# Optimization experiments

Hardware: AMD Instinct MI355X
Metric: run time of the kernel (lower is better)

The kernel has to match this reference:

```python
import jax, jax.numpy as jnp
import numpy as np

LEAK = 0.2

def leaky(x):
    return jnp.where(x > 0, x, LEAK * x)

def relu(x):
    return jnp.maximum(x, 0)

def conv1d(x, w):
    # x [B,Cin,L], w [Cout,Cin,3], stride 1, padding 1
    return jax.lax.conv_general_dilated(x, w, (1,), [(1, 1)],
        dimension_numbers=('NCH', 'OIH', 'NCH'))

def conv2d(x, w, pad, dil=1, groups=1):
    return jax.lax.conv_general_dilated(x, w, (1, 1), [(pad, pad), (pad, pad)],
        rhs_dilation=(dil, dil), feature_group_count=groups,
        dimension_numbers=('NCHW', 'OIHW', 'NCHW'))

def bn2d(x, p, eps=1e-5):
    # p: [4,C] = gamma, beta, running_mean, running_var (eval-mode BN)
    g, b, m, v = p
    s = (1, -1, 1, 1)
    return (x - m.reshape(s)) * (g.reshape(s) / jnp.sqrt(v.reshape(s) + eps)) + b.reshape(s)

def layernorm(x, g, b, eps=1e-5):
    mu = x.mean(-1, keepdims=True)
    var = ((x - mu) ** 2).mean(-1, keepdims=True)
    return (x - mu) / jnp.sqrt(var + eps) * g + b

def l2n(x, axis, eps):
    n = jnp.sqrt((x * x).sum(axis, keepdims=True))
    return x / jnp.maximum(n, eps)


def setup_inputs() -> dict:
    key = jax.random.key(0)
    B, C, H, W = 4, 64, 48, 48
    D, Fn, T, V = 256, 8, 4, 16
    E = 16  # orthogonal prototype embed dim
    ks = iter(jax.random.split(key, 64))
    def rn(shape, s=0.05):
        return jax.random.normal(next(ks), shape, jnp.float32) * s
    def bnp(c):
        return jnp.stack([1.0 + rn((c,), 0.1), rn((c,), 0.1), rn((c,), 0.1), 1.0 + jnp.abs(rn((c,), 0.1))])
    return dict(
        basis_vector_bank=jax.random.normal(next(ks), (T, V, D), jnp.float32),
        task_f=jax.random.normal(next(ks), (B, C, 16, 16), jnp.float32),
        img_f=jax.random.normal(next(ks), (B, C, H, W), jnp.float32),
        protos=jax.random.normal(next(ks), (T, E), jnp.float32),
        tA_w1=rn((E // 4, 1, 3)), tA_w2=rn((E // 2, E // 4, 3)),
        iA_w=rn((E // 2, C, 3, 3)), iA_bn=bnp(E // 2),
        at_w1=rn((E, Fn // 2 * E)), at_b1=rn((Fn // 2 * E,)),
        at_ln_g=jnp.ones((Fn // 2 * E,)), at_ln_b=jnp.zeros((Fn // 2 * E,)),
        at_w2=rn((Fn // 2 * E, Fn * E)), at_b2=rn((Fn * E,)),
        bv_t1=rn((D // 4, 1, 3)), bv_t2=rn((D // 2, D // 4, 3)),
        bv_ic1=rn((D // 4, C, 3, 3)), bv_bn1=bnp(D // 4),
        bv_ic2=rn((D // 2, D // 4, 3, 3)), bv_bn2=bnp(D // 2),
        bv_w1=rn((D, D // 4)), bv_b1=rn((D // 4,)),
        bv_ln_g=jnp.ones((D // 4,)), bv_ln_b=jnp.zeros((D // 4,)),
        bv_w2=rn((D // 4, D)), bv_b2=rn((D,)),
        m1_w1=rn((D, D // 4)), m1_b1=rn((D // 4,)),
        m1_ln_g=jnp.ones((D // 4,)), m1_ln_b=jnp.zeros((D // 4,)),
        m1_w2=rn((D // 4, C * C)), m1_b2=rn((C * C,)),
        m3_w1=rn((D, D // 4)), m3_b1=rn((D // 4,)),
        m3_ln_g=jnp.ones((D // 4,)), m3_ln_b=jnp.zeros((D // 4,)),
        m3_w2=rn((D // 4, 9 * C * C)), m3_b2=rn((9 * C * C,)),
        blr_bn=bnp(C),
        zc_w=rn((C, C, 1, 1), 0.01), zc_b=rn((C,), 0.01),
    )


def _forward(basis_vector_bank, task_f, img_f, protos, tA_w1, tA_w2, iA_w, iA_bn,
             at_w1, at_b1, at_ln_g, at_ln_b, at_w2, at_b2,
             bv_t1, bv_t2, bv_ic1, bv_bn1, bv_ic2, bv_bn2,
             bv_w1, bv_b1, bv_ln_g, bv_ln_b, bv_w2, bv_b2,
             m1_w1, m1_b1, m1_ln_g, m1_ln_b, m1_w2, m1_b2,
             m3_w1, m3_b1, m3_ln_g, m3_ln_b, m3_w2, m3_b2,
             blr_bn, zc_w, zc_b):
    T, V, D = basis_vector_bank.shape
    B, C, H, W = img_f.shape
    E = protos.shape[1]
    Fn = at_w2.shape[1] // E
    tau = 0.5

    # --- A2SI routing features ---
    xt = task_f.reshape(B, 1, -1)
    t1 = conv1d(leaky(conv1d(xt, tA_w1)), tA_w2).mean(-1)          # [B,E/2]
    i1 = leaky(bn2d(conv2d(img_f, iA_w, 1), iA_bn)).mean((2, 3))   # [B,E/2]
    f1 = jnp.concatenate([t1, i1], axis=1)                         # [B,E]
    h = relu(layernorm(f1 @ at_w1 + at_b1, at_ln_g, at_ln_b))
    tif = (h @ at_w2 + at_b2).reshape(B, E, Fn)                    # [B,E,F]
    logits = jnp.einsum('te,bef->bft', l2n(protos, -1, 1e-8), l2n(tif, 1, 1e-8))  # [B,F,T]

    # hard gumbel-softmax (straight-through), fixed noise key for determinism
    u = jax.random.uniform(jax.random.key(42), logits.shape, jnp.float32, 1e-10, 1.0)
    g = -jnp.log(-jnp.log(u))
    y = jax.nn.softmax((logits + g) / tau, axis=-1)
    idx = jnp.argmax(y, axis=-1)                                   # [B,F]
    y_hard = jax.nn.one_hot(idx, T, dtype=y.dtype)
    set_type = y_hard + y - jax.lax.stop_gradient(y)

    bank_flat = basis_vector_bank.reshape(T, V * D)
    sbvb = jnp.einsum('bft,tk->bfk', set_type, bank_flat).reshape(B, Fn, V, D)

    # --- BasisV_filter: filter feature ---
    xt2 = task_f.reshape(B, C, -1)
    rms = jnp.sqrt((xt2 ** 2).mean((1, 2), keepdims=True))
    xt2 = (xt2 / (rms + 1e-8)).reshape(B, 1, -1)
    te = conv1d(leaky(conv1d(xt2, bv_t1)), bv_t2).mean(-1)         # [B,D/2]
    ie = leaky(bn2d(conv2d(img_f, bv_ic1, 1), bv_bn1))
    ie = leaky(bn2d(conv2d(ie, bv_ic2, 1), bv_bn2)).mean((2, 3))   # [B,D/2]
    ff = jnp.concatenate([te, ie], axis=1)                         # [B,D]
    ff = relu(layernorm(ff @ bv_w1 + bv_b1, bv_ln_g, bv_ln_b)) @ bv_w2 + bv_b2

    # --- per-(batch,type) group gather/top-k/scatter, vectorized ---
    # group bank = bank of first filter with that type (hard one-hot -> type's bank)
    occ = idx[:, None, :] == jnp.arange(T)[None, :, None]          # [B,T,F]
    first = jnp.argmax(occ, axis=-1)                               # [B,T]
    Bg = jnp.take_along_axis(sbvb, first[:, :, None, None], axis=1)  # [B,T,V,D]
    # all rows of Q within a group are identical (filter_f expanded over F),
    # so S.max(0) == cosine(ff[b], Bg[b,t])
    scores = jnp.einsum('bd,btvd->btv', l2n(ff, -1, 1e-12), l2n(Bg, -1, 1e-12))
    order = jnp.argsort(-scores, axis=-1)                          # [B,T,V] topk order
    lt = jnp.tril(jnp.ones((Fn, Fn), bool), -1)                    # j < i
    rank = ((idx[:, :, None] == idx[:, None, :]) & lt).sum(-1)     # position in group
    bidx = jnp.arange(B)[:, None]
    sel = order[bidx, idx, rank]                                   # [B,F]
    bvf = Bg[bidx, idx, sel]                                       # [B,F,D]

    # --- per-filter dynamic convolutions ---
    w1 = relu(layernorm(bvf @ m1_w1 + m1_b1, m1_ln_g, m1_ln_b)) @ m1_w2 + m1_b2
    w1 = w1.reshape(B, Fn, C, C)                                   # [B,F,out,in]
    w3 = relu(layernorm(bvf @ m3_w1 + m3_b1, m3_ln_g, m3_ln_b)) @ m3_w2 + m3_b2
    w3 = w3.reshape(B * Fn, C, C, 3, 3)

    dp0 = jnp.einsum('bfoc,bchw->bfohw', w1, img_f)                # 1x1 branch
    xin = jnp.broadcast_to(img_f[:, None], (B, Fn, C, H, W)).reshape(1, B * Fn * C, H, W)
    ker = w3.reshape(B * Fn * C, C, 3, 3)
    dpd = [conv2d(xin, ker, d, dil=d, groups=B * Fn).reshape(B, Fn, C, H, W)
           for d in (1, 2, 3)]                                     # same-padded dilated 3x3
    t_ = idx[:, :, None, None, None]
    dp = jnp.where(t_ == 0, dp0, jnp.where(t_ == 1, dpd[0],
         jnp.where(t_ == 2, dpd[1], dpd[2])))                      # [B,F,C,H,W]

    x = leaky(bn2d(dp.reshape(B * Fn, C, H, W), blr_bn)).reshape(B, Fn, C, H, W).mean(1)
    a = conv2d(x, zc_w, 0) + zc_b.reshape(1, -1, 1, 1)
    return a + img_f


@jax.jit
def reference(basis_vector_bank, task_f, img_f, protos, tA_w1, tA_w2, iA_w, iA_bn,
              at_w1, at_b1, at_ln_g, at_ln_b, at_w2, at_b2,
              bv_t1, bv_t2, bv_ic1, bv_bn1, bv_ic2, bv_bn2,
              bv_w1, bv_b1, bv_ln_g, bv_ln_b, bv_w2, bv_b2,
              m1_w1, m1_b1, m1_ln_g, m1_ln_b, m1_w2, m1_b2,
              m3_w1, m3_b1, m3_ln_g, m3_ln_b, m3_w2, m3_b2,
              blr_bn, zc_w, zc_b):
    return _forward(basis_vector_bank, task_f, img_f, protos, tA_w1, tA_w2, iA_w, iA_bn,
                    at_w1, at_b1, at_ln_g, at_ln_b, at_w2, at_b2,
                    bv_t1, bv_t2, bv_ic1, bv_bn1, bv_ic2, bv_bn2,
                    bv_w1, bv_b1, bv_ln_g, bv_ln_b, bv_w2, bv_b2,
                    m1_w1, m1_b1, m1_ln_g, m1_ln_b, m1_w2, m1_b2,
                    m3_w1, m3_b1, m3_ln_g, m3_ln_b, m3_w2, m3_b2,
                    blr_bn, zc_w, zc_b)
```

## Files before the change

### kernel.cpp

```cpp
#include <hip/hip_runtime.h>
#include <math.h>

#define LEAKC 0.2f

#define NB 4
#define NC 64
#define LLEN 16384
#define HW 2304
#define PP 54
#define PHW 2916
#define SLABP 72
#define CP 72
#define IE1C 50

typedef __attribute__((ext_vector_type(8))) short short8;
typedef __attribute__((ext_vector_type(4))) float floatx4;

__device__ __forceinline__ float leaky(float x){ return x > 0.f ? x : LEAKC*x; }

__device__ __forceinline__ float wave_sum64(float v){
  for(int off=32;off;off>>=1) v += __shfl_xor(v,off);
  return v;
}

__device__ __forceinline__ unsigned short f2bf(float x){
  unsigned u=__float_as_uint(x);
  unsigned r=u+0x7FFFu+((u>>16)&1u);
  return (unsigned short)(r>>16);
}

__device__ __forceinline__ void threefry2x32(unsigned k0, unsigned k1, unsigned& x0, unsigned& x1){
  unsigned ks0=k0, ks1=k1, ks2=k0^k1^0x1BD11BDAu;
  x0+=ks0; x1+=ks1;
  const int rot0[4]={13,15,26,6};
  const int rot1[4]={17,29,16,24};
#define TF_APPLY(rr) {for(int r=0;r<4;r++){x0+=x1; x1=(x1<<rr[r])|(x1>>(32-rr[r])); x1^=x0;}}
  TF_APPLY(rot0); x0+=ks1; x1+=ks2+1u;
  TF_APPLY(rot1); x0+=ks2; x1+=ks0+2u;
  TF_APPLY(rot0); x0+=ks0; x1+=ks1+3u;
  TF_APPLY(rot1); x0+=ks1; x1+=ks2+4u;
  TF_APPLY(rot0); x0+=ks2; x1+=ks0+5u;
#undef TF_APPLY
}

__device__ __forceinline__ float jax_uniform128(int i){
  unsigned x0=0u, x1=(unsigned)i;
  threefry2x32(0u,42u,x0,x1);
  unsigned bits = x0 ^ x1;
  unsigned fb=(bits>>9)|0x3f800000u;
  float f=__uint_as_float(fb)-1.0f;
  float u=f*(1.0f-1e-10f)+1e-10f;
  return fmaxf(1e-10f,u);
}

__global__ __launch_bounds__(256) void k_pre(const float* __restrict__ task_f,
                      const float* __restrict__ w1A, const float* __restrict__ w1B,
                      float* __restrict__ totApart, float* __restrict__ a0A, float* __restrict__ aLA,
                      float* __restrict__ totBpart, float* __restrict__ a0B, float* __restrict__ aLB,
                      float* __restrict__ rmspart,
                      const float* __restrict__ img,
                      const float* __restrict__ w1, const float* __restrict__ w2,
                      const float* __restrict__ wa,
                      unsigned short* __restrict__ imgTP,
                      unsigned short* __restrict__ W1T, unsigned short* __restrict__ W2T,
                      unsigned short* __restrict__ WAT,
                      const float* __restrict__ mw1, const float* __restrict__ mw3,
                      const float* __restrict__ bvw1p, const float* __restrict__ bvw2p,
                      const float* __restrict__ bvt2p, const float* __restrict__ atw2p,
                      const float* __restrict__ bankp, float* __restrict__ warm){
  if(blockIdx.x<256){
    int b=blockIdx.x>>6, seg=blockIdx.x&63;
    const float* x=task_f+b*LLEN;
    float tA[4]={0,0,0,0};
    float tB[64];
#pragma unroll
    for(int c=0;c<64;c++) tB[c]=0.f;
    float sq=0.f;
    int l=seg*256+threadIdx.x;
    {
      float xm=(l>0)?x[l-1]:0.f;
      float xc=x[l];
      float xp=(l<LLEN-1)?x[l+1]:0.f;
      sq=xc*xc;
#pragma unroll
      for(int c=0;c<4;c++){
        float a=leaky(w1A[c*3+0]*xm + w1A[c*3+1]*xc + w1A[c*3+2]*xp);
        tA[c]=a;
        if(l==0) a0A[b*4+c]=a;
        if(l==LLEN-1) aLA[b*4+c]=a;
      }
#pragma unroll
      for(int c=0;c<64;c++){
        float a=leaky(w1B[c*3+0]*xm + w1B[c*3+1]*xc + w1B[c*3+2]*xp);
        tB[c]=a;
        if(l==0) a0B[b*64+c]=a;
        if(l==LLEN-1) aLB[b*64+c]=a;
      }
    }
    sq=wave_sum64(sq);
#pragma unroll
    for(int c=0;c<4;c++) tA[c]=wave_sum64(tA[c]);
#pragma unroll
    for(int c=0;c<64;c++){
      float v=tB[c];
      for(int off=32;off;off>>=1) v+=__shfl_down(v,off);
      tB[c]=v;
    }
    __shared__ float redB[4][64];
    __shared__ float redA[4][4];
    __shared__ float redQ[4];
    int wave=threadIdx.x>>6, lane=threadIdx.x&63;
    if(lane==0){
#pragma unroll
      for(int c=0;c<64;c++) redB[wave][c]=tB[c];
#pragma unroll
      for(int c=0;c<4;c++) redA[wave][c]=tA[c];
      redQ[wave]=sq;
    }
    __syncthreads();
    if(threadIdx.x<64){
      float s=redB[0][threadIdx.x]+redB[1][threadIdx.x]+redB[2][threadIdx.x]+redB[3][threadIdx.x];
      totBpart[(size_t)(b*64+seg)*64+threadIdx.x]=s;
    } else if(threadIdx.x<68){
      int c=threadIdx.x-64;
      totApart[(b*64+seg)*4+c]=redA[0][c]+redA[1][c]+redA[2][c]+redA[3][c];
    } else if(threadIdx.x==68){
      rmspart[b*64+seg]=redQ[0]+redQ[1]+redQ[2]+redQ[3];
    }
  } else if(blockIdx.x<400){
    int blk=blockIdx.x-256;
    int b=blk/36, t=blk%36;
    int p0=t*64;
    __shared__ float tile[64][65];
    int pp=threadIdx.x&63, c4=threadIdx.x>>6;
    for(int r=0;r<16;r++){
      int c=c4*16+r;
      tile[c][pp]=img[(b*64+c)*HW + p0+pp];
    }
    __syncthreads();
    int pxl=threadIdx.x>>2, cg=(threadIdx.x&3)*16;
    unsigned out[8];
#pragma unroll
    for(int q=0;q<8;q++){
      unsigned lo=f2bf(tile[cg+2*q][pxl]);
      unsigned hi=f2bf(tile[cg+2*q+1][pxl]);
      out[q]=lo|(hi<<16);
    }
    int px=p0+pxl;
    int h=px/48, w=px-h*48;
    int poff=(h+3)*PP+(w+3);
    unsigned* dst=(unsigned*)(imgTP + ((size_t)(b*PHW+poff))*64 + cg);
#pragma unroll
    for(int q=0;q<8;q++) dst[q]=out[q];
  } else if(blockIdx.x<868){
    int n=(blockIdx.x-400)*256+threadIdx.x;
    if(n<9*64*64){
      int tap=n>>12, oc=(n>>6)&63, c=n&63;
      W1T[n]=f2bf(w1[oc*576+c*9+tap]);
    } else if(n<9*64*64+9*128*64){
      int m=n-9*64*64;
      int tap=m/8192, r=m-tap*8192, oc=r>>6, c=r&63;
      W2T[m]=f2bf(w2[oc*576+c*9+tap]);
    } else {
      int q=n-9*64*64-9*128*64;
      if(q<9*16*64){
        int tap=q>>10, r=q&1023, o=r>>6, c=r&63;
        WAT[q]=(o<8)?f2bf(wa[o*576+c*9+tap]):(unsigned short)0;
      }
    }
  } else if(blockIdx.x<884){
    int t=(blockIdx.x-868)*256+threadIdx.x;
    float a=0.f;
    for(int i=t;i*16<16384;i+=4096) a+=mw1[i*16];
    for(int i=t;i*16<16384;i+=4096) a+=mw3[i*16];
    for(int i=t;i*16<16384;i+=4096) a+=bvw1p[i*16];
    for(int i=t;i*16<16384;i+=4096) a+=bvw2p[i*16];
    for(int i=t;i*16<24576;i+=4096) a+=bvt2p[i*16];
    for(int i=t;i*16<8192;i+=4096) a+=atw2p[i*16];
    for(int i=t;i*16<16384;i+=4096) a+=bankp[i*16];
    warm[t&1023]=a;
  } else {
    int id=(blockIdx.x-884)*256+threadIdx.x;
    uint4 z=make_uint4(0,0,0,0);
    for(int cch=id;cch<19584;cch+=4096){
      int ck=cch&7, pxid=cch>>3;
      int b=pxid/612, p=pxid-b*612;
      int h,w;
      if(p<324){ int r=p/54; w=p-r*54; h=(r<3)?r:(r+48); }
      else { int q=p-324; int r2=q/6; int cc=q-r2*6; h=3+r2; w=(cc<3)?cc:(cc+48); }
      *(uint4*)(imgTP + ((size_t)(b*PHW + h*PP + w))*64 + ck*8)=z;
    }
  }
}

__global__ __launch_bounds__(512) void k_conv12(const unsigned short* __restrict__ imgTP,
                        const unsigned short* __restrict__ W1T,
                        const unsigned short* __restrict__ W2T,
                        const unsigned short* __restrict__ WAT,
                        const float* __restrict__ bn1, const float* __restrict__ bn2,
                        const float* __restrict__ bnA,
                        float* __restrict__ iepart, float* __restrict__ i1part){
  int tid=threadIdx.x;
  int lane=tid&63, wv=tid>>6;
  int n0=lane&15, kg=lane>>4;
  if(blockIdx.x<96){
    int blk=blockIdx.x;
    int b=blk/24, hp=blk-b*24;
    int h0=hp*2;
    __shared__ unsigned short slab[6*54*SLABP];
    __shared__ unsigned short ie1[4*IE1C*CP];
    {
      const unsigned short* ibase=imgTP+((size_t)b*PHW+(size_t)(h0+1)*PP)*64;
      for(int e=tid;e<6*54*8;e+=512){
        int rr=e/(54*8), rem=e-rr*54*8, w=rem>>3, ck=rem&7;
        uint4 v=*(const uint4*)(ibase+((size_t)(rr*PP+w))*64+ck*8);
        *(uint4*)(slab+(rr*54+w)*SLABP+ck*8)=v;
      }
      if(tid<64){
        int br=tid>>4, cq=(tid>>3)&1, ck=tid&7;
        *(uint4*)(ie1+((size_t)(br*IE1C+(cq?49:0)))*CP+ck*8)=make_uint4(0,0,0,0);
      }
    }
    __syncthreads();
    {
      int mt=wv&3, rh=wv>>2;
      floatx4 acc[2][3];
#pragma unroll
      for(int rr=0;rr<2;rr++)
#pragma unroll
        for(int nt=0;nt<3;nt++) acc[rr][nt]=(floatx4){0.f,0.f,0.f,0.f};
#pragma unroll
      for(int ti=0;ti<3;ti++){
#pragma unroll
        for(int tj=0;tj<3;tj++){
          int tap=ti*3+tj;
          const unsigned short* Ab=W1T+(size_t)tap*4096;
#pragma unroll
          for(int c0=0;c0<64;c0+=32){
            short8 a=*(const short8*)(Ab+((mt*16+n0)*64+c0+kg*8));
#pragma unroll
            for(int rr=0;rr<2;rr++){
              int sr=rh*2+rr+ti;
#pragma unroll
              for(int nt=0;nt<3;nt++){
                int sc=nt*16+n0+tj+2;
                short8 bv=*(const short8*)(slab+(sr*54+sc)*SLABP+c0+kg*8);
                acc[rr][nt]=__builtin_amdgcn_mfma_f32_16x16x32_bf16(a,bv,acc[rr][nt],0,0,0);
              }
            }
          }
        }
      }
      int obase=mt*16+kg*4;
      float scale[4],m_[4],be_[4];
#pragma unroll
      for(int reg=0;reg<4;reg++){
        int o=obase+reg;
        scale[reg]=bn1[o]/sqrtf(bn1[192+o]+1e-5f);
        m_[reg]=bn1[128+o]; be_[reg]=bn1[64+o];
      }
#pragma unroll
      for(int rr=0;rr<2;rr++){
        int br=rh*2+rr;
        bool rv=((unsigned)(h0-1+br))<48u;
#pragma unroll
        for(int nt=0;nt<3;nt++){
          float v0=rv?leaky((acc[rr][nt][0]-m_[0])*scale[0]+be_[0]):0.f;
          float v1=rv?leaky((acc[rr][nt][1]-m_[1])*scale[1]+be_[1]):0.f;
          float v2=rv?leaky((acc[rr][nt][2]-m_[2])*scale[2]+be_[2]):0.f;
          float v3=rv?leaky((acc[rr][nt][3]-m_[3])*scale[3]+be_[3]):0.f;
          unsigned w0=f2bf(v0)|((unsigned)f2bf(v1)<<16);
          unsigned w1=f2bf(v2)|((unsigned)f2bf(v3)<<16);
          uint2 pk={w0,w1};
          *(uint2*)(ie1+((size_t)(br*IE1C+(nt*16+1+n0)))*CP+obase)=pk;
        }
      }
    }
    __syncthreads();
    {
      int mt2=wv;
      floatx4 acc[6];
#pragma unroll
      for(int i=0;i<6;i++) acc[i]=(floatx4){0.f,0.f,0.f,0.f};
#pragma unroll
      for(int ti=0;ti<3;ti++){
#pragma unroll
        for(int tj=0;tj<3;tj++){
          int tap=ti*3+tj;
          const unsigned short* Ab=W2T+(size_t)tap*8192;
#pragma unroll
          for(int c0=0;c0<64;c0+=32){
            short8 a=*(const short8*)(Ab+((mt2*16+n0)*64+c0+kg*8));
#pragma unroll
            for(int rr=0;rr<2;rr++){
              int sr=rr+ti;
#pragma unroll
              for(int wc=0;wc<3;wc++){
                int q=wc*16+n0+tj;
                short8 bv=*(const short8*)(ie1+((size_t)(sr*IE1C+q))*CP+c0+kg*8);
                acc[rr*3+wc]=__builtin_amdgcn_mfma_f32_16x16x32_bf16(a,bv,acc[rr*3+wc],0,0,0);
              }
            }
          }
        }
      }
      int obase=mt2*16+kg*4;
#pragma unroll
      for(int reg=0;reg<4;reg++){
        int o=obase+reg;
        float scale=bn2[o]/sqrtf(bn2[384+o]+1e-5f);
        float m_=bn2[256+o], be_=bn2[128+o];
        float part=0;
#pragma unroll
        for(int i=0;i<6;i++) part+=leaky((acc[i][reg]-m_)*scale+be_);
        for(int off=1;off<16;off<<=1) part+=__shfl_xor(part,off);
        if(n0==0) iepart[(b*24+hp)*128+o]=part*(1.f/2304.f);
      }
    }
  } else {
    int blk2=blockIdx.x-96;
    int b=blk2/3, hg=blk2-b*3;
    int hp=hg*8+wv;
    int h0=hp*2;
    const unsigned short* ib=imgTP+(size_t)b*PHW*64;
    floatx4 acc[6];
#pragma unroll
    for(int i=0;i<6;i++) acc[i]=(floatx4){0.f,0.f,0.f,0.f};
#pragma unroll
    for(int ti=0;ti<3;ti++){
#pragma unroll
      for(int tj=0;tj<3;tj++){
        int tap=ti*3+tj;
        const unsigned short* Ab=WAT+(size_t)tap*1024;
#pragma unroll
        for(int c0=0;c0<64;c0+=32){
          short8 a=*(const short8*)(Ab+(n0*64+c0+kg*8));
#pragma unroll
          for(int rr=0;rr<2;rr++){
            int r=h0+rr+ti-1+3;
#pragma unroll
            for(int wc=0;wc<3;wc++){
              int w=wc*16+n0+tj-1+3;
              short8 bv=*(const short8*)(ib+((size_t)(r*PP+w)*64+c0+kg*8));
              acc[rr*3+wc]=__builtin_amdgcn_mfma_f32_16x16x32_bf16(a,bv,acc[rr*3+wc],0,0,0);
            }
          }
        }
      }
    }
    int obase=kg*4;
#pragma unroll
    for(int reg=0;reg<4;reg++){
      int o=obase+reg;
      float part=0;
      if(o<8){
        float scale=bnA[o]/sqrtf(bnA[24+o]+1e-5f);
        float m_=bnA[16+o], be_=bnA[8+o];
#pragma unroll
        for(int i=0;i<6;i++) part+=leaky((acc[i][reg]-m_)*scale+be_);
      }
      for(int off=1;off<16;off<<=1) part+=__shfl_xor(part,off);
      if(n0==0 && o<8) i1part[(b*24+hp)*8+o]=part*(1.f/2304.f);
    }
  }
}

__global__ __launch_bounds__(512,1) void k_mid(
    const float* __restrict__ totApart, const float* __restrict__ a0A, const float* __restrict__ aLA,
    const float* __restrict__ totBpart, const float* __restrict__ a0B, const float* __restrict__ aLB,
    const float* __restrict__ rmspart,
    const float* __restrict__ tA_w2, const float* __restrict__ bv_t2,
    const float* __restrict__ i1part, const float* __restrict__ iepart,
    const float* __restrict__ at_w1, const float* __restrict__ at_b1,
    const float* __restrict__ at_ln_g, const float* __restrict__ at_ln_b,
    const float* __restrict__ at_w2, const float* __restrict__ at_b2,
    const float* __restrict__ protos,
    const float* __restrict__ bv_w1, const float* __restrict__ bv_b1,
    const float* __restrict__ bv_ln_g, const float* __restrict__ bv_ln_b,
    const float* __restrict__ bv_w2, const float* __restrict__ bv_b2,
    const float* __restrict__ bank,
    const float* __restrict__ m1_w1, const float* __restrict__ m1_b1,
    const float* __restrict__ m1_g,  const float* __restrict__ m1_bb,
    const float* __restrict__ m3_w1, const float* __restrict__ m3_b1,
    const float* __restrict__ m3_g,  const float* __restrict__ m3_bb,
    int* __restrict__ idxo, float* __restrict__ hid1, float* __restrict__ hid3){
  int b=blockIdx.x;
  int tid=threadIdx.x;
  int lane=tid&63, wv=tid>>6;
  const float invL=1.0f/16384.0f;
  __shared__ float sT[64], s0[64], sL[64];
  __shared__ float totA_s[4];
  __shared__ float rms_s;
  __shared__ float part[512];
  __shared__ float te_s[128], t1_s[8];
  __shared__ float f1[16], h[64], tif[128], tifn[128], tden[8], pden[4], pn[64], z[32];
  __shared__ int sidx[8], sfirst[4], srank[8], rows[8];
  __shared__ float fbuf[256], hh[64], ffn_s[256], finv_s;
  __shared__ float scores[64];
  __shared__ int order[64];
  __shared__ float bvf[2048];

  if(tid<64){
    float s=0;
#pragma unroll 8
    for(int seg=0;seg<64;seg++) s+=totBpart[(size_t)(b*64+seg)*64+tid];
    sT[tid]=s;
  } else if(tid<128){
    int t=tid-64;
    s0[t]=a0B[b*64+t]; sL[t]=aLB[b*64+t];
  } else if(tid<192){
    float v=rmspart[b*64+(tid-128)];
    v=wave_sum64(v);
    if(tid==128) rms_s=v;
  } else if(tid<256){
    int c=tid-192;
    if(c<4){
      float s=0;
#pragma unroll 8
      for(int seg=0;seg<64;seg++) s+=totApart[(b*64+seg)*4+c];
      totA_s[c]=s;
    }
  }
  __syncthreads();
  float scB=1.0f/(sqrtf(rms_s*invL)+1e-8f);
  if(tid<256){
    int c2=tid&127, h2=tid>>7;
    const float* wr=bv_t2+c2*192;
    float s=0;
    for(int c1=h2*32;c1<h2*32+32;c1+=8){
      float4 q[6];
      const float4* r4=(const float4*)(wr+c1*3);
#pragma unroll
      for(int u=0;u<6;u++) q[u]=r4[u];
      const float* qq=(const float*)q;
#pragma unroll
      for(int u=0;u<8;u++){
        int c=c1+u;
        float T=sT[c], A0=s0[c], AL=sL[c];
        s += qq[u*3+0]*(T-AL) + qq[u*3+1]*T + qq[u*3+2]*(T-A0);
      }
    }
    part[tid]=s;
  } else if(tid>=384 && tid<392){
    int c2=tid-384;
    float s=0;
    for(int c1=0;c1<4;c1++){
      float T=totA_s[c1], A0=a0A[b*4+c1], AL=aLA[b*4+c1];
      const float* w=&tA_w2[(c2*4+c1)*3];
      s += w[0]*(T-AL) + w[1]*T + w[2]*(T-A0);
    }
    t1_s[c2]=s*invL;
  }
  __syncthreads();
  if(tid<128) te_s[tid]=(part[tid]+part[tid+128])*invL*scB;
  __syncthreads();

  if(tid<8) f1[tid]=t1_s[tid];
  else if(tid<16){
    int f=tid-8;
    float s=0;
#pragma unroll
    for(int g=0;g<24;g++) s+=i1part[(b*24+g)*8+f];
    f1[tid]=s;
  }
  __syncthreads();
  if(tid<64){
    float s=at_b1[lane];
#pragma unroll
    for(int i=0;i<16;i++) s+=f1[i]*at_w1[i*64+lane];
    float mu=wave_sum64(s)*(1.f/64.f);
    float d=s-mu;
    float var=wave_sum64(d*d)*(1.f/64.f);
    h[lane]=fmaxf(d*(1.0f/sqrtf(var+1e-5f))*at_ln_g[lane]+at_ln_b[lane],0.f);
  }
  __syncthreads();
  if(tid<256){
    int n=tid&127, h2=tid>>7;
    float a0=0,a1=0;
    for(int k=h2*32;k<h2*32+32;k+=2){
      a0+=h[k]*at_w2[k*128+n];
      a1+=h[k+1]*at_w2[(k+1)*128+n];
    }
    part[tid]=a0+a1;
  }
  __syncthreads();
  if(tid<128) tif[tid]=at_b2[tid]+part[tid]+part[tid+128];
  __syncthreads();
  if(tid<8){
    int f=tid;
    float ss=0; for(int e=0;e<16;e++){float v=tif[e*8+f]; ss+=v*v;}
    tden[f]=fmaxf(sqrtf(ss),1e-8f);
  } else if(tid<12){
    int t=tid-8;
    float ss=0; for(int e=0;e<16;e++){float v=protos[t*16+e]; ss+=v*v;}
    pden[t]=fmaxf(sqrtf(ss),1e-8f);
  }
  __syncthreads();
  if(tid<128) tifn[tid]=tif[tid]/tden[tid&7];
  if(tid<64) pn[tid]=protos[tid]/pden[tid>>4];
  __syncthreads();
  if(tid<32){
    int f=tid>>2, t=tid&3;
    float ss=0;
#pragma unroll
    for(int e=0;e<16;e++) ss+=pn[t*16+e]*tifn[e*8+f];
    float u=jax_uniform128(b*32+f*4+t);
    float g=-logf(-logf(u));
    z[tid]=ss+g;
  }
  __syncthreads();
  if(tid<8){
    float best=z[tid*4]; int bi=0;
    for(int t=1;t<4;t++){ float v=z[tid*4+t]; if(v>best){best=v;bi=t;} }
    sidx[tid]=bi;
  }
  __syncthreads();
  if(tid<4){
    int t=tid;
    int fi=0;
    for(int f=7;f>=0;f--) if(sidx[f]==t) fi=f;
    sfirst[t]=fi;
  } else if(tid<12){
    int f=tid-4;
    int c=0; for(int f2=0;f2<f;f2++) if(sidx[f2]==sidx[f]) c++;
    srank[f]=c;
  }
  __syncthreads();

  if(tid<128) fbuf[tid]=te_s[tid];
  else if(tid<256){
    int c=tid-128;
    float s=0;
#pragma unroll 8
    for(int g=0;g<24;g++) s+=iepart[(b*24+g)*128+c];
    fbuf[tid]=s;
  }
  __syncthreads();
  if(tid<256){
    int l64=tid&63, q=tid>>6;
    float a0=0,a1=0,a2=0,a3=0;
    for(int k=q*64;k<q*64+64;k+=4){
      a0+=fbuf[k]  *bv_w1[k*64+l64];
      a1+=fbuf[k+1]*bv_w1[(k+1)*64+l64];
      a2+=fbuf[k+2]*bv_w1[(k+2)*64+l64];
      a3+=fbuf[k+3]*bv_w1[(k+3)*64+l64];
    }
    part[tid]=((a0+a1)+(a2+a3));
  }
  __syncthreads();
  if(tid<64){
    float s=bv_b1[lane]+part[lane]+part[64+lane]+part[128+lane]+part[192+lane];
    float mu=wave_sum64(s)*(1.f/64.f);
    float d=s-mu;
    float var=wave_sum64(d*d)*(1.f/64.f);
    hh[lane]=fmaxf(d*(1.0f/sqrtf(var+1e-5f))*bv_ln_g[lane]+bv_ln_b[lane],0.f);
  }
  __syncthreads();
  {
    int n=tid&255, h2=tid>>8;
    float a0=0,a1=0;
    for(int k=h2*32;k<h2*32+32;k+=2){
      a0+=hh[k]*bv_w2[k*256+n];
      a1+=hh[k+1]*bv_w2[(k+1)*256+n];
    }
    part[tid]=a0+a1;
  }
  __syncthreads();
  if(tid<256) ffn_s[tid]=bv_b2[tid]+part[tid]+part[tid+256];
  __syncthreads();
  if(tid<64){
    float sq=0;
#pragma unroll
    for(int u=0;u<4;u++){ float v=ffn_s[u*64+lane]; sq+=v*v; }
    sq=wave_sum64(sq);
    if(lane==0) finv_s=1.0f/fmaxf(sqrtf(sq),1e-12f);
  }
  __syncthreads();
  if(tid<256) ffn_s[tid]*=finv_s;
  __syncthreads();

  if(tid<128){
    int it=tid&63, h2=tid>>6;
    int t=it>>4, v=it&15;
    int tt=sidx[sfirst[t]];
    const float4* row=(const float4*)(bank+(tt*16+v)*256);
    float sa=0,na=0;
    for(int d4=h2*32;d4<h2*32+32;d4++){
      float4 r=row[d4];
      const float* fp=&ffn_s[d4*4];
      sa+=fp[0]*r.x+fp[1]*r.y+fp[2]*r.z+fp[3]*r.w;
      na+=r.x*r.x+r.y*r.y+r.z*r.z+r.w*r.w;
    }
    part[tid]=sa;
    part[256+tid]=na;
  }
  __syncthreads();
  if(tid<64) scores[tid]=(part[tid]+part[tid+64])/fmaxf(sqrtf(part[256+tid]+part[320+tid]),1e-12f);
  __syncthreads();
  if(tid<4){
    const float* sc=&scores[tid*16];
    unsigned used=0;
    for(int pk=0;pk<16;pk++){
      int best=-1; float bv=-1e30f;
      for(int v2=0;v2<16;v2++){
        if(used&(1u<<v2)) continue;
        float vv=sc[v2];
        if(best<0||vv>bv){bv=vv;best=v2;}
      }
      used|=1u<<best;
      order[tid*16+pk]=best;
    }
  }
  __syncthreads();
  if(tid<8){
    int t=sidx[tid];
    int v=order[t*16+srank[tid]];
    rows[tid]=t*16+v;
    idxo[b*8+tid]=t;
  }
  __syncthreads();

  for(int ii=tid;ii<2048;ii+=512){
    int r=ii>>8, d=ii&255;
    bvf[ii]=bank[rows[r]*256+d];
  }
  __syncthreads();
  {
    int r=wv;
    const float* bp=&bvf[r*256];
    float a0=0,a1=0,a2=0,a3=0;
    float c0=0,c1=0,c2=0,c3=0;
    for(int d=0;d<256;d+=4){
      float b0=bp[d],b1=bp[d+1],b2=bp[d+2],b3=bp[d+3];
      a0+=b0*m1_w1[d*64+lane];
      a1+=b1*m1_w1[(d+1)*64+lane];
      a2+=b2*m1_w1[(d+2)*64+lane];
      a3+=b3*m1_w1[(d+3)*64+lane];
      c0+=b0*m3_w1[d*64+lane];
      c1+=b1*m3_w1[(d+1)*64+lane];
      c2+=b2*m3_w1[(d+2)*64+lane];
      c3+=b3*m3_w1[(d+3)*64+lane];
    }
    float s1=m1_b1[lane]+((a0+a1)+(a2+a3));
    float s3=m3_b1[lane]+((c0+c1)+(c2+c3));
    float mu=wave_sum64(s1)*(1.f/64.f);
    float dd=s1-mu;
    float var=wave_sum64(dd*dd)*(1.f/64.f);
    hid1[(b*8+r)*64+lane]=fmaxf(dd*(1.0f/sqrtf(var+1e-5f))*m1_g[lane]+m1_bb[lane],0.f);
    mu=wave_sum64(s3)*(1.f/64.f);
    dd=s3-mu;
    var=wave_sum64(dd*dd)*(1.f/64.f);
    hid3[(b*8+r)*64+lane]=fmaxf(dd*(1.0f/sqrtf(var+1e-5f))*m3_g[lane]+m3_bb[lane],0.f);
  }
}

__global__ __launch_bounds__(256) void k_heads(const float* __restrict__ hid1, const float* __restrict__ hid3,
                        const float* __restrict__ w2a, const float* __restrict__ b2a,
                        const float* __restrict__ w2b, const float* __restrict__ b2b,
                        unsigned short* __restrict__ A1, unsigned short* __restrict__ A3){
  __shared__ float hl[2048];
  if(blockIdx.x<16){
    int n=blockIdx.x*256+threadIdx.x;
    for(int i=threadIdx.x;i<2048;i+=256) hl[i]=hid1[i];
    __syncthreads();
    float wcol[64];
#pragma unroll
    for(int k=0;k<64;k++) wcol[k]=w2a[k*4096+n];
    float bb=b2a[n];
    for(int bf=0;bf<32;bf++){
      float s=bb;
#pragma unroll
      for(int k=0;k<64;k++) s+=hl[bf*64+k]*wcol[k];
      A1[bf*4096+n]=f2bf(s);
    }
  } else {
    int n=(blockIdx.x-16)*256+threadIdx.x;
    for(int i=threadIdx.x;i<2048;i+=256) hl[i]=hid3[i];
    __syncthreads();
    float wcol[64];
#pragma unroll
    for(int k=0;k<64;k++) wcol[k]=w2b[(size_t)k*36864+n];
    float bb=b2b[n];
    int o=n/576, rem=n-o*576;
    int c=rem/9, tap=rem-c*9;
    size_t base=((size_t)tap*64+o)*64+c;
    for(int bf=0;bf<32;bf++){
      float s=bb;
#pragma unroll
      for(int k=0;k<64;k++) s+=hl[bf*64+k]*wcol[k];
      A3[(size_t)bf*9*4096+base]=f2bf(s);
    }
  }
}

__global__ __launch_bounds__(512) void k_dynF(const unsigned short* __restrict__ imgTP,
                       const unsigned short* __restrict__ A1, const unsigned short* __restrict__ A3,
                       const int* __restrict__ idx, const float* __restrict__ bn,
                       const float* __restrict__ zc_w, const float* __restrict__ zc_b,
                       const float* __restrict__ img, float* __restrict__ out){
  int blk=blockIdx.x;
  int b=blk/48, r0=blk-b*48;
  int tid=threadIdx.x;
  int lane=tid&63, w8=tid>>6;
  int mt=w8&3, fh=w8>>2;
  int n0=lane&15, kg=lane>>4;
  __shared__ unsigned short slab[7*54*SLABP];
  __shared__ float xl[64*50];
  __shared__ float zl[4096];
  for(int i=tid;i<4096;i+=512) zl[i]=zc_w[i];
  for(int i=tid;i<3200;i+=512) xl[i]=0.f;
  {
    const unsigned short* ibase=imgTP+((size_t)b*PHW+(size_t)r0*PP)*64;
    for(int e=tid;e<7*54*8;e+=512){
      int rr=e/(54*8), rem=e-rr*54*8, w=rem>>3, ck=rem&7;
      uint4 v=*(const uint4*)(ibase + ((size_t)(rr*PP+w))*64 + ck*8);
      *(uint4*)(slab + (rr*54+w)*SLABP + ck*8)=v;
    }
  }
  __syncthreads();
  int obase=mt*16+kg*4;
  float scale[4],m_[4],be_[4];
#pragma unroll
  for(int reg=0;reg<4;reg++){
    int o=obase+reg;
    scale[reg]=bn[o]/sqrtf(bn[192+o]+1e-5f);
    m_[reg]=bn[128+o]; be_[reg]=bn[64+o];
  }
  float xsum[3][4];
#pragma unroll
  for(int wc=0;wc<3;wc++)
#pragma unroll
    for(int reg=0;reg<4;reg++) xsum[wc][reg]=0.f;
  for(int f=fh*4;f<fh*4+4;f++){
    int bf=b*8+f;
    int tt=idx[bf];
    floatx4 acc[3];
#pragma unroll
    for(int i=0;i<3;i++) acc[i]=(floatx4){0.f,0.f,0.f,0.f};
    if(tt==0){
      const unsigned short* Ab=A1+(size_t)bf*4096;
#pragma unroll
      for(int c0=0;c0<64;c0+=32){
        short8 a=*(const short8*)(Ab+((mt*16+n0)*64+c0+kg*8));
#pragma unroll
        for(int wc=0;wc<3;wc++){
          short8 bv=*(const short8*)(slab + (3*54 + wc*16+n0+3)*SLABP + c0+kg*8);
          acc[wc]=__builtin_amdgcn_mfma_f32_16x16x32_bf16(a,bv,acc[wc],0,0,0);
        }
      }
    } else {
      int d=tt;
      const unsigned short* A3b=A3+(size_t)bf*9*4096;
#pragma unroll
      for(int ti=0;ti<3;ti++){
        int lr=d*(ti-1)+3;
#pragma unroll
        for(int tj=0;tj<3;tj++){
          int tap=ti*3+tj;
          int dw=d*(tj-1)+3;
          const unsigned short* Ab=A3b+(size_t)tap*4096;
#pragma unroll
          for(int c0=0;c0<64;c0+=32){
            short8 a=*(const short8*)(Ab+((mt*16+n0)*64+c0+kg*8));
#pragma unroll
            for(int wc=0;wc<3;wc++){
              short8 bv=*(const short8*)(slab + (lr*54 + wc*16+n0+dw)*SLABP + c0+kg*8);
              acc[wc]=__builtin_amdgcn_mfma_f32_16x16x32_bf16(a,bv,acc[wc],0,0,0);
            }
          }
        }
      }
    }
#pragma unroll
    for(int wc=0;wc<3;wc++)
#pragma unroll
      for(int reg=0;reg<4;reg++)
        xsum[wc][reg]+=leaky((acc[wc][reg]-m_[reg])*scale[reg]+be_[reg]);
  }
#pragma unroll
  for(int wc=0;wc<3;wc++)
#pragma unroll
    for(int reg=0;reg<4;reg++)
      atomicAdd(&xl[(obase+reg)*50 + wc*16+n0], xsum[wc][reg]*0.125f);
  __syncthreads();
  size_t base=(size_t)b*64*HW + r0*48;
  for(int e=tid;e<3072;e+=512){
    int o=e/48, px=e-o*48;
    float s=zc_b[o];
#pragma unroll
    for(int c=0;c<64;c++) s+=zl[o*64+c]*xl[c*50+px];
    size_t a=base+(size_t)o*HW+px;
    out[a]=s+img[a];
  }
}

extern "C" void kernel_launch(void* const* d_in, const int* in_sizes, int n_in,
                              void* d_out, int out_size, void* d_ws, size_t ws_size,
                              hipStream_t stream){
  const float* bank   =(const float*)d_in[0];
  const float* task_f =(const float*)d_in[1];
  const float* img_f  =(const float*)d_in[2];
  const float* protos =(const float*)d_in[3];
  const float* tA_w1  =(const float*)d_in[4];
  const float* tA_w2  =(const float*)d_in[5];
  const float* iA_w   =(const float*)d_in[6];
  const float* iA_bn  =(const float*)d_in[7];
  const float* at_w1  =(const float*)d_in[8];
  const float* at_b1  =(const float*)d_in[9];
  const float* at_ln_g=(const float*)d_in[10];
  const float* at_ln_b=(const float*)d_in[11];
  const float* at_w2  =(const float*)d_in[12];
  const float* at_b2  =(const float*)d_in[13];
  const float* bv_t1  =(const float*)d_in[14];
  const float* bv_t2  =(const float*)d_in[15];
  const float* bv_ic1 =(const float*)d_in[16];
  const float* bv_bn1 =(const float*)d_in[17];
  const float* bv_ic2 =(const float*)d_in[18];
  const float* bv_bn2 =(const float*)d_in[19];
  const float* bv_w1  =(const float*)d_in[20];
  const float* bv_b1  =(const float*)d_in[21];
  const float* bv_ln_g=(const float*)d_in[22];
  const float* bv_ln_b=(const float*)d_in[23];
  const float* bv_w2  =(const float*)d_in[24];
  const float* bv_b2  =(const float*)d_in[25];
  const float* m1_w1  =(const float*)d_in[26];
  const float* m1_b1  =(const float*)d_in[27];
  const float* m1_ln_g=(const float*)d_in[28];
  const float* m1_ln_b=(const float*)d_in[29];
  const float* m1_w2  =(const float*)d_in[30];
  const float* m1_b2  =(const float*)d_in[31];
  const float* m3_w1  =(const float*)d_in[32];
  const float* m3_b1  =(const float*)d_in[33];
  const float* m3_ln_g=(const float*)d_in[34];
  const float* m3_ln_b=(const float*)d_in[35];
  const float* m3_w2  =(const float*)d_in[36];
  const float* m3_b2  =(const float*)d_in[37];
  const float* blr_bn =(const float*)d_in[38];
  const float* zc_w   =(const float*)d_in[39];
  const float* zc_b   =(const float*)d_in[40];

  float* ws=(float*)d_ws;
  float* totApart=ws+0;
  float* a0A  =ws+1024;
  float* aLA  =ws+1040;
  float* totBpart=ws+1056;
  float* a0B  =ws+17440;
  float* aLB  =ws+17696;
  float* rmspart=ws+17952;
  float* i1part =ws+18208;
  float* iepart =ws+18976;
  int*   idxp   =(int*)(ws+31264);
  float* hid1=ws+31296;
  float* hid3=ws+33344;
  unsigned short* A1p  =(unsigned short*)(ws+35392);
  unsigned short* A3p  =(unsigned short*)(ws+100928);
  unsigned short* imgTP=(unsigned short*)(ws+690752);
  unsigned short* W1Tp =(unsigned short*)(ws+1064000);
  unsigned short* W2Tp =(unsigned short*)(ws+1082432);
  unsigned short* WATp =(unsigned short*)(ws+1119296);
  float* warm =ws+1123904;

  k_pre<<<900,256,0,stream>>>(task_f, tA_w1, bv_t1,
                              totApart, a0A, aLA, totBpart, a0B, aLB, rmspart,
                              img_f, bv_ic1, bv_ic2, iA_w, imgTP, W1Tp, W2Tp, WATp,
                              m1_w1, m3_w1, bv_w1, bv_w2, bv_t2, at_w2, bank, warm);
  k_conv12<<<108,512,0,stream>>>(imgTP, W1Tp, W2Tp, WATp, bv_bn1, bv_bn2, iA_bn,
                                 iepart, i1part);
  k_mid<<<4,512,0,stream>>>(totApart,a0A,aLA,totBpart,a0B,aLB, rmspart, tA_w2, bv_t2,
                            i1part, iepart,
                            at_w1, at_b1, at_ln_g, at_ln_b, at_w2, at_b2, protos,
                            bv_w1, bv_b1, bv_ln_g, bv_ln_b, bv_w2, bv_b2, bank,
                            m1_w1, m1_b1, m1_ln_g, m1_ln_b,
                            m3_w1, m3_b1, m3_ln_g, m3_ln_b,
                            idxp, hid1, hid3);
  k_heads<<<160,256,0,stream>>>(hid1, hid3, m1_w2, m1_b2, m3_w2, m3_b2, A1p, A3p);
  k_dynF<<<192,512,0,stream>>>(imgTP, A1p, A3p, idxp, blr_bn, zc_w, zc_b, img_f, (float*)d_out);

  (void)in_sizes; (void)n_in; (void)out_size; (void)ws_size;
}
```

Before: 267.2 us.

## Merge five kernels into two with in-kernel flag-based dependency gating

Folds the preprocessing and conv12 stages into one kernel (kA), and the mid, heads and dynamic-filter stages into another (kB). Dependencies between stages are enforced with global-memory release/acquire flags and spin-waits instead of kernel boundaries. Consumer blocks can start loading their slabs before producer results are ready, which removes launch gaps and lets tail work overlap. The spin-waits assume the producer blocks are resident or already scheduled, so they risk deadlock if occupancy is insufficient, and waiting blocks hold CU resources while they spin.

```diff
diff --git a/kernel.cpp b/kernel.cpp
--- a/kernel.cpp
+++ b/kernel.cpp
@@ -12,6 +12,7 @@
 #define SLABP 72
 #define CP 72
 #define IE1C 50
+#define MAGIC 0x1357ACE9
 
 typedef __attribute__((ext_vector_type(8))) short short8;
 typedef __attribute__((ext_vector_type(4))) float floatx4;
@@ -53,30 +54,72 @@
   return fmaxf(1e-10f,u);
 }
 
-__global__ __launch_bounds__(256) void k_pre(const float* __restrict__ task_f,
-                      const float* __restrict__ w1A, const float* __restrict__ w1B,
-                      float* __restrict__ totApart, float* __restrict__ a0A, float* __restrict__ aLA,
-                      float* __restrict__ totBpart, float* __restrict__ a0B, float* __restrict__ aLB,
-                      float* __restrict__ rmspart,
-                      const float* __restrict__ img,
-                      const float* __restrict__ w1, const float* __restrict__ w2,
-                      const float* __restrict__ wa,
-                      unsigned short* __restrict__ imgTP,
-                      unsigned short* __restrict__ W1T, unsigned short* __restrict__ W2T,
-                      unsigned short* __restrict__ WAT,
-                      const float* __restrict__ mw1, const float* __restrict__ mw3,
-                      const float* __restrict__ bvw1p, const float* __restrict__ bvw2p,
-                      const float* __restrict__ bvt2p, const float* __restrict__ atw2p,
-                      const float* __restrict__ bankp, float* __restrict__ warm){
-  if(blockIdx.x<256){
-    int b=blockIdx.x>>6, seg=blockIdx.x&63;
+__device__ __forceinline__ void gate_slots(int* slots, int nsl, int tid){
+  if(tid<nsl){
+    while(__hip_atomic_load(&slots[tid], __ATOMIC_ACQUIRE, __HIP_MEMORY_SCOPE_AGENT)!=MAGIC)
+      __builtin_amdgcn_s_sleep(8);
+  }
+  __syncthreads();
+}
+
+__device__ __forceinline__ void mark_slot(int* slot, int tid){
+  __syncthreads();
+  if(tid==0) __hip_atomic_store(slot, MAGIC, __ATOMIC_RELEASE, __HIP_MEMORY_SCOPE_AGENT);
+}
+
+__device__ __forceinline__ void gate_cnt(int* cnt, int target, int tid){
+  if(tid==0){
+    while(__hip_atomic_load(cnt, __ATOMIC_ACQUIRE, __HIP_MEMORY_SCOPE_AGENT)<target)
+      __builtin_amdgcn_s_sleep(8);
+  }
+  __syncthreads();
+}
+
+struct MidSM {
+  float sT[64], s0[64], sL[64];
+  float totA_s[4]; float rms_s;
+  float part[512];
+  float te_s[128], t1_s[8];
+  float f1[16], h[64], tif[128], tifn[128], tden[8], pden[4], pn[64], z[32];
+  int sidx[8], sfirst[4], srank[8], rows[8];
+  float fbuf[256], hh[64], ffn_s[256], finv_s;
+  float scores[64];
+  int order[64];
+  float bvf[2048];
+};
+
+__global__ __launch_bounds__(512) void kA(
+    const float* __restrict__ task_f,
+    const float* __restrict__ w1A, const float* __restrict__ w1B,
+    float* __restrict__ totApart, float* __restrict__ a0A, float* __restrict__ aLA,
+    float* __restrict__ totBpart, float* __restrict__ a0B, float* __restrict__ aLB,
+    float* __restrict__ rmspart,
+    const float* __restrict__ img,
+    const float* __restrict__ w1, const float* __restrict__ w2, const float* __restrict__ wa,
+    unsigned short* __restrict__ imgTP,
+    unsigned short* __restrict__ W1T, unsigned short* __restrict__ W2T, unsigned short* __restrict__ WAT,
+    const float* __restrict__ mw1, const float* __restrict__ mw3,
+    const float* __restrict__ bvw1p, const float* __restrict__ bvw2p,
+    const float* __restrict__ bvt2p, const float* __restrict__ atw2p,
+    const float* __restrict__ bankp, float* __restrict__ warm,
+    const float* __restrict__ bn1, const float* __restrict__ bn2, const float* __restrict__ bnA,
+    float* __restrict__ iepart, float* __restrict__ i1part,
+    int* __restrict__ slotA, int* __restrict__ bflags){
+  __shared__ __align__(16) char smraw[75456];
+  int tid=threadIdx.x;
+  int lane=tid&63, wv=tid>>6;
+  int n0=lane&15, kg=lane>>4;
+  int blk=blockIdx.x;
+
+  if(blk<128){
+    int b=blk>>5, half=tid>>8, seg=(blk&31)*2+half, t256=tid&255;
     const float* x=task_f+b*LLEN;
     float tA[4]={0,0,0,0};
     float tB[64];
 #pragma unroll
     for(int c=0;c<64;c++) tB[c]=0.f;
     float sq=0.f;
-    int l=seg*256+threadIdx.x;
+    int l=seg*256+t256;
     {
       float xm=(l>0)?x[l-1]:0.f;
       float xc=x[l];
@@ -106,39 +149,39 @@
       for(int off=32;off;off>>=1) v+=__shfl_down(v,off);
       tB[c]=v;
     }
-    __shared__ float redB[4][64];
-    __shared__ float redA[4][4];
-    __shared__ float redQ[4];
-    int wave=threadIdx.x>>6, lane=threadIdx.x&63;
+    float (*redB)[64]=(float(*)[64])smraw;
+    float (*redA)[4]=(float(*)[4])(smraw+2048);
+    float *redQ=(float*)(smraw+2048+128);
     if(lane==0){
 #pragma unroll
-      for(int c=0;c<64;c++) redB[wave][c]=tB[c];
-#pragma unroll
-      for(int c=0;c<4;c++) redA[wave][c]=tA[c];
-      redQ[wave]=sq;
-    }
-    __syncthreads();
-    if(threadIdx.x<64){
-      float s=redB[0][threadIdx.x]+redB[1][threadIdx.x]+redB[2][threadIdx.x]+redB[3][threadIdx.x];
-      totBpart[(size_t)(b*64+seg)*64+threadIdx.x]=s;
-    } else if(threadIdx.x<68){
-      int c=threadIdx.x-64;
-      totApart[(b*64+seg)*4+c]=redA[0][c]+redA[1][c]+redA[2][c]+redA[3][c];
-    } else if(threadIdx.x==68){
-      rmspart[b*64+seg]=redQ[0]+redQ[1]+redQ[2]+redQ[3];
-    }
-  } else if(blockIdx.x<400){
-    int blk=blockIdx.x-256;
-    int b=blk/36, t=blk%36;
+      for(int c=0;c<64;c++) redB[wv][c]=tB[c];
+#pragma unroll
+      for(int c=0;c<4;c++) redA[wv][c]=tA[c];
+      redQ[wv]=sq;
+    }
+    __syncthreads();
+    int w0=half*4;
+    if(t256<64){
+      float s=redB[w0][t256]+redB[w0+1][t256]+redB[w0+2][t256]+redB[w0+3][t256];
+      totBpart[(size_t)(b*64+seg)*64+t256]=s;
+    } else if(t256<68){
+      int c=t256-64;
+      totApart[(b*64+seg)*4+c]=redA[w0][c]+redA[w0+1][c]+redA[w0+2][c]+redA[w0+3][c];
+    } else if(t256==68){
+      rmspart[b*64+seg]=redQ[w0]+redQ[w0+1]+redQ[w0+2]+redQ[w0+3];
+    }
+  } else if(blk<200){
+    int j=blk-128, b=j/18, pr=j-b*18, half=tid>>8, t=pr*2+half, t256=tid&255;
+    float (*tile2)[64][65]=(float(*)[64][65])smraw;
+    float (*tile)[65]=tile2[half];
     int p0=t*64;
-    __shared__ float tile[64][65];
-    int pp=threadIdx.x&63, c4=threadIdx.x>>6;
+    int pp=t256&63, c4=t256>>6;
     for(int r=0;r<16;r++){
       int c=c4*16+r;
       tile[c][pp]=img[(b*64+c)*HW + p0+pp];
     }
     __syncthreads();
-    int pxl=threadIdx.x>>2, cg=(threadIdx.x&3)*16;
+    int pxl=t256>>2, cg=(t256&3)*16;
     unsigned out[8];
 #pragma unroll
     for(int q=0;q<8;q++){
@@ -152,24 +195,25 @@
     unsigned* dst=(unsigned*)(imgTP + ((size_t)(b*PHW+poff))*64 + cg);
 #pragma unroll
     for(int q=0;q<8;q++) dst[q]=out[q];
-  } else if(blockIdx.x<868){
-    int n=(blockIdx.x-400)*256+threadIdx.x;
-    if(n<9*64*64){
-      int tap=n>>12, oc=(n>>6)&63, c=n&63;
-      W1T[n]=f2bf(w1[oc*576+c*9+tap]);
-    } else if(n<9*64*64+9*128*64){
-      int m=n-9*64*64;
-      int tap=m/8192, r=m-tap*8192, oc=r>>6, c=r&63;
-      W2T[m]=f2bf(w2[oc*576+c*9+tap]);
-    } else {
-      int q=n-9*64*64-9*128*64;
-      if(q<9*16*64){
+    mark_slot(&slotA[j], tid);
+  } else if(blk<230){
+    for(int n=(blk-200)*512+tid;n<119808;n+=15360){
+      if(n<36864){
+        int tap=n>>12, oc=(n>>6)&63, c=n&63;
+        W1T[n]=f2bf(w1[oc*576+c*9+tap]);
+      } else if(n<110592){
+        int m=n-36864;
+        int tap=m/8192, r=m-tap*8192, oc=r>>6, c=r&63;
+        W2T[m]=f2bf(w2[oc*576+c*9+tap]);
+      } else {
+        int q=n-110592;
         int tap=q>>10, r=q&1023, o=r>>6, c=r&63;
         WAT[q]=(o<8)?f2bf(wa[o*576+c*9+tap]):(unsigned short)0;
       }
     }
-  } else if(blockIdx.x<884){
-    int t=(blockIdx.x-868)*256+threadIdx.x;
+    mark_slot(&slotA[72+(blk-200)], tid);
+  } else if(blk<238){
+    int t=(blk-230)*512+tid;
     float a=0.f;
     for(int i=t;i*16<16384;i+=4096) a+=mw1[i*16];
     for(int i=t;i*16<16384;i+=4096) a+=mw3[i*16];
@@ -179,8 +223,10 @@
     for(int i=t;i*16<8192;i+=4096) a+=atw2p[i*16];
     for(int i=t;i*16<16384;i+=4096) a+=bankp[i*16];
     warm[t&1023]=a;
-  } else {
-    int id=(blockIdx.x-884)*256+threadIdx.x;
+  } else if(blk<246){
+    int hb=blk-238;
+    if(hb==0 && tid<2) __hip_atomic_store(&bflags[tid],0,__ATOMIC_RELAXED,__HIP_MEMORY_SCOPE_AGENT);
+    int id=hb*512+tid;
     uint4 z=make_uint4(0,0,0,0);
     for(int cch=id;cch<19584;cch+=4096){
       int ck=cch&7, pxid=cch>>3;
@@ -190,25 +236,14 @@
       else { int q=p-324; int r2=q/6; int cc=q-r2*6; h=3+r2; w=(cc<3)?cc:(cc+48); }
       *(uint4*)(imgTP + ((size_t)(b*PHW + h*PP + w))*64 + ck*8)=z;
     }
-  }
-}
-
-__global__ __launch_bounds__(512) void k_conv12(const unsigned short* __restrict__ imgTP,
-                        const unsigned short* __restrict__ W1T,
-                        const unsigned short* __restrict__ W2T,
-                        const unsigned short* __restrict__ WAT,
-                        const float* __restrict__ bn1, const float* __restrict__ bn2,
-                        const float* __restrict__ bnA,
-                        float* __restrict__ iepart, float* __restrict__ i1part){
-  int tid=threadIdx.x;
-  int lane=tid&63, wv=tid>>6;
-  int n0=lane&15, kg=lane>>4;
-  if(blockIdx.x<96){
-    int blk=blockIdx.x;
-    int b=blk/24, hp=blk-b*24;
+    mark_slot(&slotA[102+hb], tid);
+  } else if(blk<342){
+    gate_slots(slotA,110,tid);
+    int cblk=blk-246;
+    int b=cblk/24, hp=cblk-b*24;
     int h0=hp*2;
-    __shared__ unsigned short slab[6*54*SLABP];
-    __shared__ unsigned short ie1[4*IE1C*CP];
+    unsigned short* slab=(unsigned short*)smraw;
+    unsigned short* ie1=(unsigned short*)(smraw+46656);
     {
       const unsigned short* ibase=imgTP+((size_t)b*PHW+(size_t)(h0+1)*PP)*64;
       for(int e=tid;e<6*54*8;e+=512){
@@ -270,8 +305,8 @@
           float v2=rv?leaky((acc[rr][nt][2]-m_[2])*scale[2]+be_[2]):0.f;
           float v3=rv?leaky((acc[rr][nt][3]-m_[3])*scale[3]+be_[3]):0.f;
           unsigned w0=f2bf(v0)|((unsigned)f2bf(v1)<<16);
-          unsigned w1=f2bf(v2)|((unsigned)f2bf(v3)<<16);
-          uint2 pk={w0,w1};
+          unsigned w1p=f2bf(v2)|((unsigned)f2bf(v3)<<16);
+          uint2 pk={w0,w1p};
           *(uint2*)(ie1+((size_t)(br*IE1C+(nt*16+1+n0)))*CP+obase)=pk;
         }
       }
@@ -318,8 +353,9 @@
       }
     }
   } else {
-    int blk2=blockIdx.x-96;
-    int b=blk2/3, hg=blk2-b*3;
+    gate_slots(slotA,110,tid);
+    int ablk=blk-342;
+    int b=ablk/3, hg=ablk%3;
     int hp=hg*8+wv;
     int h0=hp*2;
     const unsigned short* ib=imgTP+(size_t)b*PHW*64;
@@ -365,7 +401,7 @@
   }
 }
 
-__global__ __launch_bounds__(512,1) void k_mid(
+__global__ __launch_bounds__(512,1) void kB(
     const float* __restrict__ totApart, const float* __restrict__ a0A, const float* __restrict__ aLA,
     const float* __restrict__ totBpart, const float* __restrict__ a0B, const float* __restrict__ aLB,
     const float* __restrict__ rmspart,
@@ -383,414 +419,423 @@
     const float* __restrict__ m1_g,  const float* __restrict__ m1_bb,
     const float* __restrict__ m3_w1, const float* __restrict__ m3_b1,
     const float* __restrict__ m3_g,  const float* __restrict__ m3_bb,
-    int* __restrict__ idxo, float* __restrict__ hid1, float* __restrict__ hid3){
-  int b=blockIdx.x;
+    int* __restrict__ idxo, float* __restrict__ hid1, float* __restrict__ hid3,
+    const float* __restrict__ w2a, const float* __restrict__ b2a,
+    const float* __restrict__ w2b, const float* __restrict__ b2b,
+    unsigned short* __restrict__ A1, unsigned short* __restrict__ A3,
+    const unsigned short* __restrict__ imgTP, const float* __restrict__ bnD,
+    const float* __restrict__ zc_w, const float* __restrict__ zc_b,
+    const float* __restrict__ img, float* __restrict__ out,
+    float* __restrict__ warm, int* __restrict__ bflags){
+  __shared__ __align__(16) char smraw[83616];
   int tid=threadIdx.x;
   int lane=tid&63, wv=tid>>6;
-  const float invL=1.0f/16384.0f;
-  __shared__ float sT[64], s0[64], sL[64];
-  __shared__ float totA_s[4];
-  __shared__ float rms_s;
-  __shared__ float part[512];
-  __shared__ float te_s[128], t1_s[8];
-  __shared__ float f1[16], h[64], tif[128], tifn[128], tden[8], pden[4], pn[64], z[32];
-  __shared__ int sidx[8], sfirst[4], srank[8], rows[8];
-  __shared__ float fbuf[256], hh[64], ffn_s[256], finv_s;
-  __shared__ float scores[64];
-  __shared__ int order[64];
-  __shared__ float bvf[2048];
-
-  if(tid<64){
-    float s=0;
-#pragma unroll 8
-    for(int seg=0;seg<64;seg++) s+=totBpart[(size_t)(b*64+seg)*64+tid];
-    sT[tid]=s;
-  } else if(tid<128){
-    int t=tid-64;
-    s0[t]=a0B[b*64+t]; sL[t]=aLB[b*64+t];
-  } else if(tid<192){
-    float v=rmspart[b*64+(tid-128)];
-    v=wave_sum64(v);
-    if(tid==128) rms_s=v;
-  } else if(tid<256){
-    int c=tid-192;
-    if(c<4){
+  int blk=blockIdx.x;
+
+  if(blk<4){
+    MidSM* S=(MidSM*)smraw;
+    int b=blk;
+    const float invL=1.0f/16384.0f;
+    if(tid<64){
       float s=0;
 #pragma unroll 8
-      for(int seg=0;seg<64;seg++) s+=totApart[(b*64+seg)*4+c];
-      totA_s[c]=s;
-    }
-  }
-  __syncthreads();
-  float scB=1.0f/(sqrtf(rms_s*invL)+1e-8f);
-  if(tid<256){
-    int c2=tid&127, h2=tid>>7;
-    const float* wr=bv_t2+c2*192;
-    float s=0;
-    for(int c1=h2*32;c1<h2*32+32;c1+=8){
-      float4 q[6];
-      const float4* r4=(const float4*)(wr+c1*3);
-#pragma unroll
-      for(int u=0;u<6;u++) q[u]=r4[u];
-      const float* qq=(const float*)q;
-#pragma unroll
-      for(int u=0;u<8;u++){
-        int c=c1+u;
-        float T=sT[c], A0=s0[c], AL=sL[c];
-        s += qq[u*3+0]*(T-AL) + qq[u*3+1]*T + qq[u*3+2]*(T-A0);
-      }
-    }
-    part[tid]=s;
-  } else if(tid>=384 && tid<392){
-    int c2=tid-384;
-    float s=0;
-    for(int c1=0;c1<4;c1++){
-      float T=totA_s[c1], A0=a0A[b*4+c1], AL=aLA[b*4+c1];
-      const float* w=&tA_w2[(c2*4+c1)*3];
-      s += w[0]*(T-AL) + w[1]*T + w[2]*(T-A0);
-    }
-    t1_s[c2]=s*invL;
-  }
-  __syncthreads();
-  if(tid<128) te_s[tid]=(part[tid]+part[tid+128])*invL*scB;
-  __syncthreads();
-
-  if(tid<8) f1[tid]=t1_s[tid];
-  else if(tid<16){
-    int f=tid-8;
-    float s=0;
-#pragma unroll
-    for(int g=0;g<24;g++) s+=i1part[(b*24+g)*8+f];
-    f1[tid]=s;
-  }
-  __syncthreads();
-  if(tid<64){
-    float s=at_b1[lane];
-#pragma unroll
-    for(int i=0;i<16;i++) s+=f1[i]*at_w1[i*64+lane];
-    float mu=wave_sum64(s)*(1.f/64.f);
-    float d=s-mu;
-    float var=wave_sum64(d*d)*(1.f/64.f);
-    h[lane]=fmaxf(d*(1.0f/sqrtf(var+1e-5f))*at_ln_g[lane]+at_ln_b[lane],0.f);
-  }
-  __syncthreads();
-  if(tid<256){
-    int n=tid&127, h2=tid>>7;
-    float a0=0,a1=0;
-    for(int k=h2*32;k<h2*32+32;k+=2){
-      a0+=h[k]*at_w2[k*128+n];
-      a1+=h[k+1]*at_w2[(k+1)*128+n];
-    }
-    part[tid]=a0+a1;
-  }
-  __syncthreads();
-  if(tid<128) tif[tid]=at_b2[tid]+part[tid]+part[tid+128];
-  __syncthreads();
-  if(tid<8){
-    int f=tid;
-    float ss=0; for(int e=0;e<16;e++){float v=tif[e*8+f]; ss+=v*v;}
-    tden[f]=fmaxf(sqrtf(ss),1e-8f);
-  } else if(tid<12){
-    int t=tid-8;
-    float ss=0; for(int e=0;e<16;e++){float v=protos[t*16+e]; ss+=v*v;}
-    pden[t]=fmaxf(sqrtf(ss),1e-8f);
-  }
-  __syncthreads();
-  if(tid<128) tifn[tid]=tif[tid]/tden[tid&7];
-  if(tid<64) pn[tid]=protos[tid]/pden[tid>>4];
-  __syncthreads();
-  if(tid<32){
-    int f=tid>>2, t=tid&3;
-    float ss=0;
-#pragma unroll
-    for(int e=0;e<16;e++) ss+=pn[t*16+e]*tifn[e*8+f];
-    float u=jax_uniform128(b*32+f*4+t);
-    float g=-logf(-logf(u));
-    z[tid]=ss+g;
-  }
-  __syncthreads();
-  if(tid<8){
-    float best=z[tid*4]; int bi=0;
-    for(int t=1;t<4;t++){ float v=z[tid*4+t]; if(v>best){best=v;bi=t;} }
-    sidx[tid]=bi;
-  }
-  __syncthreads();
-  if(tid<4){
-    int t=tid;
-    int fi=0;
-    for(int f=7;f>=0;f--) if(sidx[f]==t) fi=f;
-    sfirst[t]=fi;
-  } else if(tid<12){
-    int f=tid-4;
-    int c=0; for(int f2=0;f2<f;f2++) if(sidx[f2]==sidx[f]) c++;
-    srank[f]=c;
-  }
-  __syncthreads();
-
-  if(tid<128) fbuf[tid]=te_s[tid];
-  else if(tid<256){
-    int c=tid-128;
-    float s=0;
+      for(int seg=0;seg<64;seg++) s+=totBpart[(size_t)(b*64+seg)*64+tid];
+      S->sT[tid]=s;
+    } else if(tid<128){
+      int t=tid-64;
+      S->s0[t]=a0B[b*64+t]; S->sL[t]=aLB[b*64+t];
+    } else if(tid<192){
+      float v=rmspart[b*64+(tid-128)];
+      v=wave_sum64(v);
+      if(tid==128) S->rms_s=v;
+    } else if(tid<256){
+      int c=tid-192;
+      if(c<4){
+        float s=0;
 #pragma unroll 8
-    for(int g=0;g<24;g++) s+=iepart[(b*24+g)*128+c];
-    fbuf[tid]=s;
-  }
-  __syncthreads();
-  if(tid<256){
-    int l64=tid&63, q=tid>>6;
-    float a0=0,a1=0,a2=0,a3=0;
-    for(int k=q*64;k<q*64+64;k+=4){
-      a0+=fbuf[k]  *bv_w1[k*64+l64];
-      a1+=fbuf[k+1]*bv_w1[(k+1)*64+l64];
-      a2+=fbuf[k+2]*bv_w1[(k+2)*64+l64];
-      a3+=fbuf[k+3]*bv_w1[(k+3)*64+l64];
-    }
-    part[tid]=((a0+a1)+(a2+a3));
-  }
-  __syncthreads();
-  if(tid<64){
-    float s=bv_b1[lane]+part[lane]+part[64+lane]+part[128+lane]+part[192+lane];
-    float mu=wave_sum64(s)*(1.f/64.f);
-    float d=s-mu;
-    float var=wave_sum64(d*d)*(1.f/64.f);
-    hh[lane]=fmaxf(d*(1.0f/sqrtf(var+1e-5f))*bv_ln_g[lane]+bv_ln_b[lane],0.f);
-  }
-  __syncthreads();
-  {
-    int n=tid&255, h2=tid>>8;
-    float a0=0,a1=0;
-    for(int k=h2*32;k<h2*32+32;k+=2){
-      a0+=hh[k]*bv_w2[k*256+n];
-      a1+=hh[k+1]*bv_w2[(k+1)*256+n];
-    }
-    part[tid]=a0+a1;
-  }
-  __syncthreads();
-  if(tid<256) ffn_s[tid]=bv_b2[tid]+part[tid]+part[tid+256];
-  __syncthreads();
-  if(tid<64){
-    float sq=0;
-#pragma unroll
-    for(int u=0;u<4;u++){ float v=ffn_s[u*64+lane]; sq+=v*v; }
-    sq=wave_sum64(sq);
-    if(lane==0) finv_s=1.0f/fmaxf(sqrtf(sq),1e-12f);
-  }
-  __syncthreads();
-  if(tid<256) ffn_s[tid]*=finv_s;
-  __syncthreads();
-
-  if(tid<128){
-    int it=tid&63, h2=tid>>6;
-    int t=it>>4, v=it&15;
-    int tt=sidx[sfirst[t]];
-    const float4* row=(const float4*)(bank+(tt*16+v)*256);
-    float sa=0,na=0;
-    for(int d4=h2*32;d4<h2*32+32;d4++){
-      float4 r=row[d4];
-      const float* fp=&ffn_s[d4*4];
-      sa+=fp[0]*r.x+fp[1]*r.y+fp[2]*r.z+fp[3]*r.w;
-      na+=r.x*r.x+r.y*r.y+r.z*r.z+r.w*r.w;
-    }
-    part[tid]=sa;
-    part[256+tid]=na;
-  }
-  __syncthreads();
-  if(tid<64) scores[tid]=(part[tid]+part[tid+64])/fmaxf(sqrtf(part[256+tid]+part[320+tid]),1e-12f);
-  __syncthreads();
-  if(tid<4){
-    const float* sc=&scores[tid*16];
-    unsigned used=0;
-    for(int pk=0;pk<16;pk++){
-      int best=-1; float bv=-1e30f;
-      for(int v2=0;v2<16;v2++){
-        if(used&(1u<<v2)) continue;
-        float vv=sc[v2];
-        if(best<0||vv>bv){bv=vv;best=v2;}
-      }
-      used|=1u<<best;
-      order[tid*16+pk]=best;
-    }
-  }
-  __syncthreads();
-  if(tid<8){
-    int t=sidx[tid];
-    int v=order[t*16+srank[tid]];
-    rows[tid]=t*16+v;
-    idxo[b*8+tid]=t;
-  }
-  __syncthreads();
-
-  for(int ii=tid;ii<2048;ii+=512){
-    int r=ii>>8, d=ii&255;
-    bvf[ii]=bank[rows[r]*256+d];
-  }
-  __syncthreads();
-  {
-    int r=wv;
-    const float* bp=&bvf[r*256];
-    float a0=0,a1=0,a2=0,a3=0;
-    float c0=0,c1=0,c2=0,c3=0;
-    for(int d=0;d<256;d+=4){
-      float b0=bp[d],b1=bp[d+1],b2=bp[d+2],b3=bp[d+3];
-      a0+=b0*m1_w1[d*64+lane];
-      a1+=b1*m1_w1[(d+1)*64+lane];
-      a2+=b2*m1_w1[(d+2)*64+lane];
-      a3+=b3*m1_w1[(d+3)*64+lane];
-      c0+=b0*m3_w1[d*64+lane];
-      c1+=b1*m3_w1[(d+1)*64+lane];
-      c2+=b2*m3_w1[(d+2)*64+lane];
-      c3+=b3*m3_w1[(d+3)*64+lane];
-    }
-    float s1=m1_b1[lane]+((a0+a1)+(a2+a3));
-    float s3=m3_b1[lane]+((c0+c1)+(c2+c3));
-    float mu=wave_sum64(s1)*(1.f/64.f);
-    float dd=s1-mu;
-    float var=wave_sum64(dd*dd)*(1.f/64.f);
-    hid1[(b*8+r)*64+lane]=fmaxf(dd*(1.0f/sqrtf(var+1e-5f))*m1_g[lane]+m1_bb[lane],0.f);
-    mu=wave_sum64(s3)*(1.f/64.f);
-    dd=s3-mu;
-    var=wave_sum64(dd*dd)*(1.f/64.f);
-    hid3[(b*8+r)*64+lane]=fmaxf(dd*(1.0f/sqrtf(var+1e-5f))*m3_g[lane]+m3_bb[lane],0.f);
-  }
-}
-
-__global__ __launch_bounds__(256) void k_heads(const float* __restrict__ hid1, const float* __restrict__ hid3,
-                        const float* __restrict__ w2a, const float* __restrict__ b2a,
-                        const float* __restrict__ w2b, const float* __restrict__ b2b,
-                        unsigned short* __restrict__ A1, unsigned short* __restrict__ A3){
-  __shared__ float hl[2048];
-  if(blockIdx.x<16){
-    int n=blockIdx.x*256+threadIdx.x;
-    for(int i=threadIdx.x;i<2048;i+=256) hl[i]=hid1[i];
-    __syncthreads();
-    float wcol[64];
-#pragma unroll
-    for(int k=0;k<64;k++) wcol[k]=w2a[k*4096+n];
-    float bb=b2a[n];
-    for(int bf=0;bf<32;bf++){
-      float s=bb;
-#pragma unroll
-      for(int k=0;k<64;k++) s+=hl[bf*64+k]*wcol[k];
-      A1[bf*4096+n]=f2bf(s);
-    }
+        for(int seg=0;seg<64;seg++) s+=totApart[(b*64+seg)*4+c];
+        S->totA_s[c]=s;
+      }
+    } else {
+      int t=tid-256;
+      float acc=0.f;
+      for(int i=t;i<1024;i+=256) acc+=m1_w1[i*16]+m3_w1[i*16]+bv_w2[i*16]+bank[i*16];
+      for(int i=t;i<512;i+=256) acc+=at_w2[i*16];
+      if(t<256) acc+=bv_w1[t*16];
+      warm[b*256+t]=acc;
+    }
+    __syncthreads();
+    float scB=1.0f/(sqrtf(S->rms_s*invL)+1e-8f);
+    if(tid<256){
+      int c2=tid&127, h2=tid>>7;
+      const float* wr=bv_t2+c2*192;
+      float s=0;
+      for(int c1=h2*32;c1<h2*32+32;c1+=8){
+        float4 q[6];
+        const float4* r4=(const float4*)(wr+c1*3);
+#pragma unroll
+        for(int u=0;u<6;u++) q[u]=r4[u];
+        const float* qq=(const float*)q;
+#pragma unroll
+        for(int u=0;u<8;u++){
+          int c=c1+u;
+          float T=S->sT[c], A0=S->s0[c], AL=S->sL[c];
+          s += qq[u*3+0]*(T-AL) + qq[u*3+1]*T + qq[u*3+2]*(T-A0);
+        }
+      }
+      S->part[tid]=s;
+    } else if(tid>=384 && tid<392){
+      int c2=tid-384;
+      float s=0;
+      for(int c1=0;c1<4;c1++){
+        float T=S->totA_s[c1], A0=a0A[b*4+c1], AL=aLA[b*4+c1];
+        const float* w=&tA_w2[(c2*4+c1)*3];
+        s += w[0]*(T-AL) + w[1]*T + w[2]*(T-A0);
+      }
+      S->t1_s[c2]=s*invL;
+    }
+    __syncthreads();
+    if(tid<128) S->te_s[tid]=(S->part[tid]+S->part[tid+128])*invL*scB;
+    __syncthreads();
+
+    if(tid<8) S->f1[tid]=S->t1_s[tid];
+    else if(tid<16){
+      int f=tid-8;
+      float s=0;
+#pragma unroll
+      for(int g=0;g<24;g++) s+=i1part[(b*24+g)*8+f];
+      S->f1[tid]=s;
+    }
+    __syncthreads();
+    if(tid<64){
+      float s=at_b1[lane];
+#pragma unroll
+      for(int i=0;i<16;i++) s+=S->f1[i]*at_w1[i*64+lane];
+      float mu=wave_sum64(s)*(1.f/64.f);
+      float d=s-mu;
+      float var=wave_sum64(d*d)*(1.f/64.f);
+      S->h[lane]=fmaxf(d*(1.0f/sqrtf(var+1e-5f))*at_ln_g[lane]+at_ln_b[lane],0.f);
+    }
+    __syncthreads();
+    if(tid<256){
+      int n=tid&127, h2=tid>>7;
+      float a0=0,a1=0;
+      for(int k=h2*32;k<h2*32+32;k+=2){
+        a0+=S->h[k]*at_w2[k*128+n];
+        a1+=S->h[k+1]*at_w2[(k+1)*128+n];
+      }
+      S->part[tid]=a0+a1;
+    }
+    __syncthreads();
+    if(tid<128) S->tif[tid]=at_b2[tid]+S->part[tid]+S->part[tid+128];
+    __syncthreads();
+    if(tid<8){
+      int f=tid;
+      float ss=0; for(int e=0;e<16;e++){float v=S->tif[e*8+f]; ss+=v*v;}
+      S->tden[f]=fmaxf(sqrtf(ss),1e-8f);
+    } else if(tid<12){
+      int t=tid-8;
+      float ss=0; for(int e=0;e<16;e++){float v=protos[t*16+e]; ss+=v*v;}
+      S->pden[t]=fmaxf(sqrtf(ss),1e-8f);
+    }
+    __syncthreads();
+    if(tid<128) S->tifn[tid]=S->tif[tid]/S->tden[tid&7];
+    if(tid<64) S->pn[tid]=protos[tid]/S->pden[tid>>4];
+    __syncthreads();
+    if(tid<32){
+      int f=tid>>2, t=tid&3;
+      float ss=0;
+#pragma unroll
+      for(int e=0;e<16;e++) ss+=S->pn[t*16+e]*S->tifn[e*8+f];
+      float u=jax_uniform128(b*32+f*4+t);
+      float g=-logf(-logf(u));
+      S->z[tid]=ss+g;
+    }
+    __syncthreads();
+    if(tid<8){
+      float best=S->z[tid*4]; int bi=0;
+      for(int t=1;t<4;t++){ float v=S->z[tid*4+t]; if(v>best){best=v;bi=t;} }
+      S->sidx[tid]=bi;
+    }
+    __syncthreads();
+    if(tid<4){
+      int t=tid;
+      int fi=0;
+      for(int f=7;f>=0;f--) if(S->sidx[f]==t) fi=f;
+      S->sfirst[t]=fi;
+    } else if(tid<12){
+      int f=tid-4;
+      int c=0; for(int f2=0;f2<f;f2++) if(S->sidx[f2]==S->sidx[f]) c++;
+      S->srank[f]=c;
+    }
+    __syncthreads();
+
+    if(tid<128) S->fbuf[tid]=S->te_s[tid];
+    else if(tid<256){
+      int c=tid-128;
+      float s=0;
+#pragma unroll 8
+      for(int g=0;g<24;g++) s+=iepart[(b*24+g)*128+c];
+      S->fbuf[tid]=s;
+    }
+    __syncthreads();
+    if(tid<256){
+      int l64=tid&63, q=tid>>6;
+      float a0=0,a1=0,a2=0,a3=0;
+      for(int k=q*64;k<q*64+64;k+=4){
+        a0+=S->fbuf[k]  *bv_w1[k*64+l64];
+        a1+=S->fbuf[k+1]*bv_w1[(k+1)*64+l64];
+        a2+=S->fbuf[k+2]*bv_w1[(k+2)*64+l64];
+        a3+=S->fbuf[k+3]*bv_w1[(k+3)*64+l64];
+      }
+      S->part[tid]=((a0+a1)+(a2+a3));
+    }
+    __syncthreads();
+    if(tid<64){
+      float s=bv_b1[lane]+S->part[lane]+S->part[64+lane]+S->part[128+lane]+S->part[192+lane];
+      float mu=wave_sum64(s)*(1.f/64.f);
+      float d=s-mu;
+      float var=wave_sum64(d*d)*(1.f/64.f);
+      S->hh[lane]=fmaxf(d*(1.0f/sqrtf(var+1e-5f))*bv_ln_g[lane]+bv_ln_b[lane],0.f);
+    }
+    __syncthreads();
+    {
+      int n=tid&255, h2=tid>>8;
+      float a0=0,a1=0;
+      for(int k=h2*32;k<h2*32+32;k+=2){
+        a0+=S->hh[k]*bv_w2[k*256+n];
+        a1+=S->hh[k+1]*bv_w2[(k+1)*256+n];
+      }
+      S->part[tid]=a0+a1;
+    }
+    __syncthreads();
+    if(tid<256) S->ffn_s[tid]=bv_b2[tid]+S->part[tid]+S->part[tid+256];
+    __syncthreads();
+    if(tid<64){
+      float sq=0;
+#pragma unroll
+      for(int u=0;u<4;u++){ float v=S->ffn_s[u*64+lane]; sq+=v*v; }
+      sq=wave_sum64(sq);
+      if(lane==0) S->finv_s=1.0f/fmaxf(sqrtf(sq),1e-12f);
+    }
+    __syncthreads();
+    if(tid<256) S->ffn_s[tid]*=S->finv_s;
+    __syncthreads();
+
+    if(tid<128){
+      int it=tid&63, h2=tid>>6;
+      int t=it>>4, v=it&15;
+      int tt=S->sidx[S->sfirst[t]];
+      const float4* row=(const float4*)(bank+(tt*16+v)*256);
+      float sa=0,na=0;
+      for(int d4=h2*32;d4<h2*32+32;d4++){
+        float4 r=row[d4];
+        const float* fp=&S->ffn_s[d4*4];
+        sa+=fp[0]*r.x+fp[1]*r.y+fp[2]*r.z+fp[3]*r.w;
+        na+=r.x*r.x+r.y*r.y+r.z*r.z+r.w*r.w;
+      }
+      S->part[tid]=sa;
+      S->part[256+tid]=na;
+    }
+    __syncthreads();
+    if(tid<64) S->scores[tid]=(S->part[tid]+S->part[tid+64])/fmaxf(sqrtf(S->part[256+tid]+S->part[320+tid]),1e-12f);
+    __syncthreads();
+    if(tid<4){
+      const float* sc=&S->scores[tid*16];
+      unsigned used=0;
+      for(int pk=0;pk<16;pk++){
+        int best=-1; float bv=-1e30f;
+        for(int v2=0;v2<16;v2++){
+          if(used&(1u<<v2)) continue;
+          float vv=sc[v2];
+          if(best<0||vv>bv){bv=vv;best=v2;}
+        }
+        used|=1u<<best;
+        S->order[tid*16+pk]=best;
+      }
+    }
+    __syncthreads();
+    if(tid<8){
+      int t=S->sidx[tid];
+      int v=S->order[t*16+S->srank[tid]];
+      S->rows[tid]=t*16+v;
+      idxo[b*8+tid]=t;
+    }
+    __syncthreads();
+
+    for(int ii=tid;ii<2048;ii+=512){
+      int r=ii>>8, d=ii&255;
+      S->bvf[ii]=bank[S->rows[r]*256+d];
+    }
+    __syncthreads();
+    {
+      int r=wv;
+      const float* bp=&S->bvf[r*256];
+      float a0=0,a1=0,a2=0,a3=0;
+      float c0=0,c1=0,c2=0,c3=0;
+      for(int d=0;d<256;d+=4){
+        float b0=bp[d],b1=bp[d+1],b2=bp[d+2],b3=bp[d+3];
+        a0+=b0*m1_w1[d*64+lane];
+        a1+=b1*m1_w1[(d+1)*64+lane];
+        a2+=b2*m1_w1[(d+2)*64+lane];
+        a3+=b3*m1_w1[(d+3)*64+lane];
+        c0+=b0*m3_w1[d*64+lane];
+        c1+=b1*m3_w1[(d+1)*64+lane];
+        c2+=b2*m3_w1[(d+2)*64+lane];
+        c3+=b3*m3_w1[(d+3)*64+lane];
+      }
+      float s1=m1_b1[lane]+((a0+a1)+(a2+a3));
+      float s3=m3_b1[lane]+((c0+c1)+(c2+c3));
+      float mu=wave_sum64(s1)*(1.f/64.f);
+      float dd=s1-mu;
+      float var=wave_sum64(dd*dd)*(1.f/64.f);
+      hid1[(b*8+r)*64+lane]=fmaxf(dd*(1.0f/sqrtf(var+1e-5f))*m1_g[lane]+m1_bb[lane],0.f);
+      mu=wave_sum64(s3)*(1.f/64.f);
+      dd=s3-mu;
+      var=wave_sum64(dd*dd)*(1.f/64.f);
+      hid3[(b*8+r)*64+lane]=fmaxf(dd*(1.0f/sqrtf(var+1e-5f))*m3_g[lane]+m3_bb[lane],0.f);
+    }
+    __syncthreads();
+    if(tid==0) __hip_atomic_fetch_add(&bflags[0],1,__ATOMIC_RELEASE,__HIP_MEMORY_SCOPE_AGENT);
+  } else if(blk<44){
+    int hblk=blk-4;
+    bool a1blk = hblk<4;
+    int nA=hblk*1024+tid, nB=nA+512;
+    float wcolA[64], wcolB[64];
+    float bbA, bbB;
+    int mA=0,mB=0;
+    if(a1blk){
+#pragma unroll
+      for(int k=0;k<64;k++){ wcolA[k]=w2a[k*4096+nA]; wcolB[k]=w2a[k*4096+nB]; }
+      bbA=b2a[nA]; bbB=b2a[nB];
+    } else {
+      mA=nA-4096; mB=nB-4096;
+#pragma unroll
+      for(int k=0;k<64;k++){ wcolA[k]=w2b[(size_t)k*36864+mA]; wcolB[k]=w2b[(size_t)k*36864+mB]; }
+      bbA=b2b[mA]; bbB=b2b[mB];
+    }
+    gate_cnt(&bflags[0],4,tid);
+    float* hl=(float*)smraw;
+    const float* hsrc=a1blk?hid1:hid3;
+    for(int i=tid;i<2048;i+=512) hl[i]=hsrc[i];
+    __syncthreads();
+    if(a1blk){
+      for(int bf=0;bf<32;bf++){
+        float sA=bbA, sB=bbB;
+#pragma unroll
+        for(int k=0;k<64;k++){ float hv=hl[bf*64+k]; sA+=hv*wcolA[k]; sB+=hv*wcolB[k]; }
+        A1[bf*4096+nA]=f2bf(sA);
+        A1[bf*4096+nB]=f2bf(sB);
+      }
+    } else {
+      int oA=mA/576, remA=mA-oA*576, cA=remA/9, tapA=remA-cA*9;
+      int oB=mB/576, remB=mB-oB*576, cB=remB/9, tapB=remB-cB*9;
+      size_t baseA=((size_t)tapA*64+oA)*64+cA;
+      size_t baseB=((size_t)tapB*64+oB)*64+cB;
+      for(int bf=0;bf<32;bf++){
+        float sA=bbA, sB=bbB;
+#pragma unroll
+        for(int k=0;k<64;k++){ float hv=hl[bf*64+k]; sA+=hv*wcolA[k]; sB+=hv*wcolB[k]; }
+        A3[(size_t)bf*9*4096+baseA]=f2bf(sA);
+        A3[(size_t)bf*9*4096+baseB]=f2bf(sB);
+      }
+    }
+    __syncthreads();
+    if(tid==0) __hip_atomic_fetch_add(&bflags[1],1,__ATOMIC_RELEASE,__HIP_MEMORY_SCOPE_AGENT);
   } else {
-    int n=(blockIdx.x-16)*256+threadIdx.x;
-    for(int i=threadIdx.x;i<2048;i+=256) hl[i]=hid3[i];
-    __syncthreads();
-    float wcol[64];
-#pragma unroll
-    for(int k=0;k<64;k++) wcol[k]=w2b[(size_t)k*36864+n];
-    float bb=b2b[n];
-    int o=n/576, rem=n-o*576;
-    int c=rem/9, tap=rem-c*9;
-    size_t base=((size_t)tap*64+o)*64+c;
-    for(int bf=0;bf<32;bf++){
-      float s=bb;
-#pragma unroll
-      for(int k=0;k<64;k++) s+=hl[bf*64+k]*wcol[k];
-      A3[(size_t)bf*9*4096+base]=f2bf(s);
-    }
-  }
-}
-
-__global__ __launch_bounds__(512) void k_dynF(const unsigned short* __restrict__ imgTP,
-                       const unsigned short* __restrict__ A1, const unsigned short* __restrict__ A3,
-                       const int* __restrict__ idx, const float* __restrict__ bn,
-                       const float* __restrict__ zc_w, const float* __restrict__ zc_b,
-                       const float* __restrict__ img, float* __restrict__ out){
-  int blk=blockIdx.x;
-  int b=blk/48, r0=blk-b*48;
-  int tid=threadIdx.x;
-  int lane=tid&63, w8=tid>>6;
-  int mt=w8&3, fh=w8>>2;
-  int n0=lane&15, kg=lane>>4;
-  __shared__ unsigned short slab[7*54*SLABP];
-  __shared__ float xl[64*50];
-  __shared__ float zl[4096];
-  for(int i=tid;i<4096;i+=512) zl[i]=zc_w[i];
-  for(int i=tid;i<3200;i+=512) xl[i]=0.f;
-  {
-    const unsigned short* ibase=imgTP+((size_t)b*PHW+(size_t)r0*PP)*64;
-    for(int e=tid;e<7*54*8;e+=512){
-      int rr=e/(54*8), rem=e-rr*54*8, w=rem>>3, ck=rem&7;
-      uint4 v=*(const uint4*)(ibase + ((size_t)(rr*PP+w))*64 + ck*8);
-      *(uint4*)(slab + (rr*54+w)*SLABP + ck*8)=v;
-    }
-  }
-  __syncthreads();
-  int obase=mt*16+kg*4;
-  float scale[4],m_[4],be_[4];
-#pragma unroll
-  for(int reg=0;reg<4;reg++){
-    int o=obase+reg;
-    scale[reg]=bn[o]/sqrtf(bn[192+o]+1e-5f);
-    m_[reg]=bn[128+o]; be_[reg]=bn[64+o];
-  }
-  float xsum[3][4];
-#pragma unroll
-  for(int wc=0;wc<3;wc++)
-#pragma unroll
-    for(int reg=0;reg<4;reg++) xsum[wc][reg]=0.f;
-  for(int f=fh*4;f<fh*4+4;f++){
-    int bf=b*8+f;
-    int tt=idx[bf];
-    floatx4 acc[3];
-#pragma unroll
-    for(int i=0;i<3;i++) acc[i]=(floatx4){0.f,0.f,0.f,0.f};
-    if(tt==0){
-      const unsigned short* Ab=A1+(size_t)bf*4096;
-#pragma unroll
-      for(int c0=0;c0<64;c0+=32){
-        short8 a=*(const short8*)(Ab+((mt*16+n0)*64+c0+kg*8));
-#pragma unroll
-        for(int wc=0;wc<3;wc++){
-          short8 bv=*(const short8*)(slab + (3*54 + wc*16+n0+3)*SLABP + c0+kg*8);
-          acc[wc]=__builtin_amdgcn_mfma_f32_16x16x32_bf16(a,bv,acc[wc],0,0,0);
+    int dblk=blk-44;
+    int b=dblk/48, r0=dblk-b*48;
+    int w8=tid>>6;
+    int mt=w8&3, fh=w8>>2;
+    int n0=lane&15, kg=lane>>4;
+    unsigned short* slab=(unsigned short*)smraw;
+    float* xl=(float*)(smraw+54432);
+    float* zl=(float*)(smraw+54432+12800);
+    for(int i=tid;i<4096;i+=512) zl[i]=zc_w[i];
+    for(int i=tid;i<3200;i+=512) xl[i]=0.f;
+    {
+      const unsigned short* ibase=imgTP+((size_t)b*PHW+(size_t)r0*PP)*64;
+      for(int e=tid;e<7*54*8;e+=512){
+        int rr=e/(54*8), rem=e-rr*54*8, w=rem>>3, ck=rem&7;
+        uint4 v=*(const uint4*)(ibase + ((size_t)(rr*PP+w))*64 + ck*8);
+        *(uint4*)(slab + (rr*54+w)*SLABP + ck*8)=v;
+      }
+    }
+    gate_cnt(&bflags[1],40,tid);
+    int obase=mt*16+kg*4;
+    float scale[4],m_[4],be_[4];
+#pragma unroll
+    for(int reg=0;reg<4;reg++){
+      int o=obase+reg;
+      scale[reg]=bnD[o]/sqrtf(bnD[192+o]+1e-5f);
+      m_[reg]=bnD[128+o]; be_[reg]=bnD[64+o];
+    }
+    float xsum[3][4];
+#pragma unroll
+    for(int wc=0;wc<3;wc++)
+#pragma unroll
+      for(int reg=0;reg<4;reg++) xsum[wc][reg]=0.f;
+    for(int f=fh*4;f<fh*4+4;f++){
+      int bf=b*8+f;
+      int tt=idxo[bf];
+      floatx4 acc[3];
+#pragma unroll
+      for(int i=0;i<3;i++) acc[i]=(floatx4){0.f,0.f,0.f,0.f};
+      if(tt==0){
+        const unsigned short* Ab=A1+(size_t)bf*4096;
+#pragma unroll
+        for(int c0=0;c0<64;c0+=32){
+          short8 a=*(const short8*)(Ab+((mt*16+n0)*64+c0+kg*8));
+#pragma unroll
+          for(int wc=0;wc<3;wc++){
+            short8 bv=*(const short8*)(slab + (3*54 + wc*16+n0+3)*SLABP + c0+kg*8);
+            acc[wc]=__builtin_amdgcn_mfma_f32_16x16x32_bf16(a,bv,acc[wc],0,0,0);
+          }
         }
-      }
-    } else {
-      int d=tt;
-      const unsigned short* A3b=A3+(size_t)bf*9*4096;
-#pragma unroll
-      for(int ti=0;ti<3;ti++){
-        int lr=d*(ti-1)+3;
-#pragma unroll
-        for(int tj=0;tj<3;tj++){
-          int tap=ti*3+tj;
-          int dw=d*(tj-1)+3;
-          const unsigned short* Ab=A3b+(size_t)tap*4096;
-#pragma unroll
-          for(int c0=0;c0<64;c0+=32){
-            short8 a=*(const short8*)(Ab+((mt*16+n0)*64+c0+kg*8));
-#pragma unroll
-            for(int wc=0;wc<3;wc++){
-              short8 bv=*(const short8*)(slab + (lr*54 + wc*16+n0+dw)*SLABP + c0+kg*8);
-              acc[wc]=__builtin_amdgcn_mfma_f32_16x16x32_bf16(a,bv,acc[wc],0,0,0);
+      } else {
+        int d=tt;
+        const unsigned short* A3b=A3+(size_t)bf*9*4096;
+#pragma unroll
+        for(int ti=0;ti<3;ti++){
+          int lr=d*(ti-1)+3;
+#pragma unroll
+          for(int tj=0;tj<3;tj++){
+            int tap=ti*3+tj;
+            int dw=d*(tj-1)+3;
+            const unsigned short* Ab=A3b+(size_t)tap*4096;
+#pragma unroll
+            for(int c0=0;c0<64;c0+=32){
+              short8 a=*(const short8*)(Ab+((mt*16+n0)*64+c0+kg*8));
+#pragma unroll
+              for(int wc=0;wc<3;wc++){
+                short8 bv=*(const short8*)(slab + (lr*54 + wc*16+n0+dw)*SLABP + c0+kg*8);
+                acc[wc]=__builtin_amdgcn_mfma_f32_16x16x32_bf16(a,bv,acc[wc],0,0,0);
+              }
             }
           }
         }
       }
+#pragma unroll
+      for(int wc=0;wc<3;wc++)
+#pragma unroll
+        for(int reg=0;reg<4;reg++)
+          xsum[wc][reg]+=leaky((acc[wc][reg]-m_[reg])*scale[reg]+be_[reg]);
     }
 #pragma unroll
     for(int wc=0;wc<3;wc++)
 #pragma unroll
       for(int reg=0;reg<4;reg++)
-        xsum[wc][reg]+=leaky((acc[wc][reg]-m_[reg])*scale[reg]+be_[reg]);
-  }
-#pragma unroll
-  for(int wc=0;wc<3;wc++)
-#pragma unroll
-    for(int reg=0;reg<4;reg++)
-      atomicAdd(&xl[(obase+reg)*50 + wc*16+n0], xsum[wc][reg]*0.125f);
-  __syncthreads();
-  size_t base=(size_t)b*64*HW + r0*48;
-  for(int e=tid;e<3072;e+=512){
-    int o=e/48, px=e-o*48;
-    float s=zc_b[o];
-#pragma unroll
-    for(int c=0;c<64;c++) s+=zl[o*64+c]*xl[c*50+px];
-    size_t a=base+(size_t)o*HW+px;
-    out[a]=s+img[a];
+        atomicAdd(&xl[(obase+reg)*50 + wc*16+n0], xsum[wc][reg]*0.125f);
+    __syncthreads();
+    size_t base=(size_t)b*64*HW + r0*48;
+    for(int e=tid;e<3072;e+=512){
+      int o=e/48, px=e-o*48;
+      float s=zc_b[o];
+#pragma unroll
+      for(int c=0;c<64;c++) s+=zl[o*64+c]*xl[c*50+px];
+      size_t a=base+(size_t)o*HW+px;
+      out[a]=s+img[a];
+    }
   }
 }
 
@@ -859,22 +904,27 @@
   unsigned short* W2Tp =(unsigned short*)(ws+1082432);
   unsigned short* WATp =(unsigned short*)(ws+1119296);
   float* warm =ws+1123904;
-
-  k_pre<<<900,256,0,stream>>>(task_f, tA_w1, bv_t1,
-                              totApart, a0A, aLA, totBpart, a0B, aLB, rmspart,
-                              img_f, bv_ic1, bv_ic2, iA_w, imgTP, W1Tp, W2Tp, WATp,
-                              m1_w1, m3_w1, bv_w1, bv_w2, bv_t2, at_w2, bank, warm);
-  k_conv12<<<108,512,0,stream>>>(imgTP, W1Tp, W2Tp, WATp, bv_bn1, bv_bn2, iA_bn,
-                                 iepart, i1part);
-  k_mid<<<4,512,0,stream>>>(totApart,a0A,aLA,totBpart,a0B,aLB, rmspart, tA_w2, bv_t2,
-                            i1part, iepart,
-                            at_w1, at_b1, at_ln_g, at_ln_b, at_w2, at_b2, protos,
-                            bv_w1, bv_b1, bv_ln_g, bv_ln_b, bv_w2, bv_b2, bank,
-                            m1_w1, m1_b1, m1_ln_g, m1_ln_b,
-                            m3_w1, m3_b1, m3_ln_g, m3_ln_b,
-                            idxp, hid1, hid3);
-  k_heads<<<160,256,0,stream>>>(hid1, hid3, m1_w2, m1_b2, m3_w2, m3_b2, A1p, A3p);
-  k_dynF<<<192,512,0,stream>>>(imgTP, A1p, A3p, idxp, blr_bn, zc_w, zc_b, img_f, (float*)d_out);
+  int*   slotA=(int*)(ws+1124928);
+  int*   bflags=(int*)(ws+1125040);
+
+  kA<<<354,512,0,stream>>>(task_f, tA_w1, bv_t1,
+                           totApart, a0A, aLA, totBpart, a0B, aLB, rmspart,
+                           img_f, bv_ic1, bv_ic2, iA_w,
+                           imgTP, W1Tp, W2Tp, WATp,
+                           m1_w1, m3_w1, bv_w1, bv_w2, bv_t2, at_w2, bank, warm,
+                           bv_bn1, bv_bn2, iA_bn,
+                           iepart, i1part, slotA, bflags);
+  kB<<<236,512,0,stream>>>(totApart,a0A,aLA,totBpart,a0B,aLB, rmspart, tA_w2, bv_t2,
+                           i1part, iepart,
+                           at_w1, at_b1, at_ln_g, at_ln_b, at_w2, at_b2, protos,
+                           bv_w1, bv_b1, bv_ln_g, bv_ln_b, bv_w2, bv_b2, bank,
+                           m1_w1, m1_b1, m1_ln_g, m1_ln_b,
+                           m3_w1, m3_b1, m3_ln_g, m3_ln_b,
+                           idxp, hid1, hid3,
+                           m1_w2, m1_b2, m3_w2, m3_b2,
+                           A1p, A3p,
+                           imgTP, blr_bn, zc_w, zc_b, img_f, (float*)d_out,
+                           warm, bflags);
 
   (void)in_sizes; (void)n_in; (void)out_size; (void)ws_size;
 }
```

Result: slower. 377.0 us (+41.1%).
